# Kernel tuning notes

Measured on AMD Instinct MI355X. Metric: run time of the kernel, lower is better.

The kernel has to match this reference:

```python
import jax, jax.numpy as jnp
import numpy as np

B, S, D, V = 2, 4096, 2048, 32000
H, HD = 16, 128          # heads, head dim (H*HD == D)
BS = 16                  # block_size
N_ANCH = 128             # num_anchors (static: loss_mask=ones guarantees enough valid positions)
MASK_ID = 31999
DFF = 8192


def rms(x, w, eps=1e-6):
    return x * jax.lax.rsqrt(jnp.mean(x * x, axis=-1, keepdims=True) + eps) * w


def rope(x, pos):
    # x: (..., L, H, hd), pos: (..., L)
    hd = x.shape[-1]
    inv = 1.0 / (10000.0 ** (jnp.arange(0, hd, 2, dtype=jnp.float32) / hd))
    ang = pos[..., None, None].astype(jnp.float32) * inv  # (..., L, 1, hd/2)
    cos, sin = jnp.cos(ang), jnp.sin(ang)
    x1, x2 = x[..., : hd // 2], x[..., hd // 2 :]
    return jnp.concatenate([x1 * cos - x2 * sin, x2 * cos + x1 * sin], axis=-1).astype(x.dtype)


def setup_inputs() -> dict:
    key = jax.random.key(0)
    ks = jax.random.split(key, 12)
    s = 0.02
    return {
        "input_ids": jax.random.randint(ks[0], (B, S), 0, V, dtype=jnp.int32),
        "hidden_states": jax.random.normal(ks[1], (B, S, D), dtype=jnp.float32),
        "loss_mask": jnp.ones((B, S), dtype=jnp.float32),
        "rand_vals": jax.random.uniform(ks[2], (B, S - BS + 1), dtype=jnp.float32),
        "embed_table": jax.random.normal(ks[3], (V, D), dtype=jnp.float32) * s,
        "lm_head_w": jax.random.normal(ks[4], (V, D), dtype=jnp.float32) * s,
        "wq": jax.random.normal(ks[5], (D, D), dtype=jnp.float32) * s,
        "wk": jax.random.normal(ks[6], (D, D), dtype=jnp.float32) * s,
        "wv": jax.random.normal(ks[7], (D, D), dtype=jnp.float32) * s,
        "wo": jax.random.normal(ks[8], (D, D), dtype=jnp.float32) * s,
        "w_gate": jax.random.normal(ks[9], (D, DFF), dtype=jnp.float32) * s,
        "w_up": jax.random.normal(ks[10], (D, DFF), dtype=jnp.float32) * s,
        "w_down": jax.random.normal(ks[11], (DFF, D), dtype=jnp.float32) * s,
        "norm_attn": jnp.ones((D,), dtype=jnp.float32),
        "norm_mlp": jnp.ones((D,), dtype=jnp.float32),
        "norm_out": jnp.ones((D,), dtype=jnp.float32),
        "norm_chs": jnp.ones((D,), dtype=jnp.float32),
    }


def reference(input_ids, hidden_states, loss_mask, rand_vals, embed_table, lm_head_w,
              wq, wk, wv, wo, w_gate, w_up, w_down, norm_attn, norm_mlp, norm_out, norm_chs):
    max_anchor = S - BS
    # ---- anchor sampling: random permutation of valid positions via argsort of rand ----
    valid = loss_mask[:, : max_anchor + 1] > 0.5                       # (B, max_anchor+1)
    valid_counts = valid.sum(axis=1)
    idx = jnp.arange(max_anchor + 1, dtype=jnp.int32)
    masked_idx = jnp.where(valid, idx[None, :], S + 1)
    rv = jnp.where(valid, rand_vals, 2.0)
    order = jnp.argsort(rv, axis=1)
    gathered = jnp.take_along_axis(masked_idx, order, axis=1)
    anchors = jnp.sort(gathered[:, :N_ANCH], axis=1)                   # (B, N)
    keep = jnp.arange(N_ANCH)[None, :] < jnp.minimum(valid_counts, N_ANCH)[:, None]
    anchors = jnp.where(keep, anchors, 0)
    # ---- noise embedding: anchor token at block start, mask token elsewhere ----
    anchor_tok = jnp.take_along_axis(input_ids, jnp.clip(anchors, 0, S - 1), axis=1)
    first_tok = jnp.where(keep, anchor_tok, MASK_ID)
    noise_ids = jnp.full((B, N_ANCH, BS), MASK_ID, dtype=jnp.int32).at[:, :, 0].set(first_tok)
    x = embed_table[noise_ids]                                         # (B,N,BS,D)
    # ---- CHS context hidden: target hidden at anchor-1 ----
    ctx_pos = jnp.maximum(anchors - 1, 0)
    ctx = jnp.take_along_axis(hidden_states, ctx_pos[:, :, None], axis=1)  # (B,N,D)
    # ---- block-diagonal attention: per-block kv = [CHS_i | draft block i] (kv_len=1+BS) ----
    pos_q = anchors[:, :, None] + jnp.arange(BS)[None, None, :]        # (B,N,BS)
    pos_kv = jnp.concatenate([ctx_pos[:, :, None], pos_q], axis=2)     # (B,N,1+BS)
    hq = rms(x, norm_attn)
    hc = rms(ctx, norm_chs)[:, :, None, :]
    kv_in = jnp.concatenate([hc, hq], axis=2)                          # (B,N,1+BS,D)
    q = rope((hq @ wq).reshape(B, N_ANCH, BS, H, HD), pos_q)
    k = rope((kv_in @ wk).reshape(B, N_ANCH, 1 + BS, H, HD), pos_kv)
    v = (kv_in @ wv).reshape(B, N_ANCH, 1 + BS, H, HD)
    scores = jnp.einsum('bnqhd,bnkhd->bnhqk', q, k) * (1.0 / HD ** 0.5)
    attn = jax.nn.softmax(scores, axis=-1)
    out = jnp.einsum('bnhqk,bnkhd->bnqhd', attn, v).reshape(B, N_ANCH, BS, D) @ wo
    out = out * keep[:, :, None, None].astype(out.dtype)               # invalid blocks fully masked
    x = x + out
    h = rms(x, norm_mlp)
    x = x + (jax.nn.silu(h @ w_gate) * (h @ w_up)) @ w_down
    h_out = rms(x, norm_out)
    logits = h_out @ lm_head_w.T                                       # (B,N,BS,V)
    # ---- block-wise CE loss ----
    label_idx = anchors[:, :, None] + jnp.arange(BS)[None, None, :]
    valid_label = label_idx < S
    safe = jnp.minimum(label_idx, S - 1)
    targets = jnp.take_along_axis(jnp.broadcast_to(input_ids[:, None, :], (B, N_ANCH, S)), safe, axis=2)
    lm_g = jnp.take_along_axis(jnp.broadcast_to(loss_mask[:, None, :], (B, N_ANCH, S)), safe, axis=2)
    weight = (keep[:, :, None] & valid_label).astype(jnp.float32)
    weight = weight * (jnp.arange(BS) > 0)[None, None, :].astype(jnp.float32) * lm_g
    logp = jax.nn.log_softmax(logits, axis=-1)
    tok_logp = jnp.take_along_axis(logp, targets[..., None].astype(jnp.int32), axis=-1)[..., 0]
    loss = -(tok_logp * weight).sum() / (weight.sum() + 1e-6)
    pred = jnp.argmax(logits, axis=-1)
    accuracy = ((pred == targets) & (weight > 0.5)).sum().astype(jnp.float32) / (weight.sum() + 1e-6)
    return loss, accuracy
```

## Files before the change

### kernel.cpp

```cpp
#include <hip/hip_runtime.h>
#include <math.h>

typedef unsigned short u16;
typedef unsigned char u8;
typedef short v8s __attribute__((ext_vector_type(8)));
typedef u16   v4u __attribute__((ext_vector_type(4)));
typedef float v4f __attribute__((ext_vector_type(4)));
typedef int   v2i __attribute__((ext_vector_type(2)));
typedef int   v4i __attribute__((ext_vector_type(4)));

#define DEVFN static __device__ __forceinline__

constexpr int cB = 2, cS = 4096, cD = 2048, cV = 32000, cH = 16, cHD = 128;
constexpr int cBS = 16, cNA = 128, cMASK = 31999, cDFF = 8192;
constexpr int NCAND = cS - cBS + 1;
constexpr int MTOK  = cB * cNA * cBS;
constexpr int MKV   = cB * cNA * 17;
constexpr int NCH   = cV / 128;
constexpr int NCH2  = cV / 256;

constexpr int EPI_BF16 = 0, EPI_SILU = 1, EPI_OEMB = 2, EPI_DOWNACC = 3, EPI_STATS = 4, EPI_GLU = 5;
constexpr int ASRC_BF16 = 0, ASRC_RMS = 1, ASRC_AOMAP = 2;

struct RmsSrc {
  const float* hs; const float* emb; const float* nattn; const float* nchs;
  const float* rowinv; const int* ftok; const int* cpos;
};

DEVFN u16 f2bf(float f) {
  union { float f; unsigned u; } a; a.f = f;
  unsigned u = a.u;
  u = u + 0x7fffu + ((u >> 16) & 1u);
  return (u16)(u >> 16);
}
DEVFN float bf2f(u16 h) {
  union { unsigned u; float f; } a; a.u = ((unsigned)h) << 16;
  return a.f;
}
DEVFN float waveSum(float v) {
  #pragma unroll
  for (int o = 32; o >= 1; o >>= 1) v += __shfl_xor(v, o);
  return v;
}
DEVFN void gload16(void* lds, const void* g) {
  __builtin_amdgcn_global_load_lds(
      (const __attribute__((address_space(1))) unsigned*)g,
      (__attribute__((address_space(3))) unsigned*)lds, 16, 0, 0);
}
DEVFN int pack4fp8(float a, float b, float c, float d) {
  int p = __builtin_amdgcn_cvt_pk_fp8_f32(a, b, 0, 0);
  p = __builtin_amdgcn_cvt_pk_fp8_f32(c, d, p, 1);
  return p;
}
DEVFN long perm8(long i) {
  return (i & ~63L) | (((i >> 3) & 3) << 4) | (((i >> 5) & 1) << 3);
}

__global__ void k_select(const float* __restrict__ lmask, const float* __restrict__ rv_in,
                         int* __restrict__ self) {
  int b = blockIdx.x >> 4, chunk = blockIdx.x & 15;
  __shared__ float rvs[4096];
  for (int i = threadIdx.x; i < NCAND; i += 256) {
    bool valid = lmask[(size_t)b * cS + i] > 0.5f;
    rvs[i] = valid ? rv_in[(size_t)b * NCAND + i] : 2.0f;
  }
  __syncthreads();
  int i = chunk * 256 + threadIdx.x;
  if (i < NCAND) {
    float v = rvs[i];
    int rank = 0;
    for (int j = 0; j < NCAND; ++j) {
      float u = rvs[j];
      rank += (u < v) || (u == v && j < i);
    }
    self[(size_t)b * NCAND + i] = (rank < cNA) ? 1 : 0;
  }
}

__global__ void k_anchors(const float* __restrict__ lmask, const int* __restrict__ self,
                          const int* __restrict__ ids, int* __restrict__ anchors,
                          int* __restrict__ keepA, int* __restrict__ ftok, int* __restrict__ cpos) {
  int b = blockIdx.x;
  __shared__ int flags[4096];
  __shared__ int ssum[256];
  __shared__ int soff[257];
  __shared__ int abuf[cNA];
  for (int i = threadIdx.x; i < 4096; i += 256)
    flags[i] = (i < NCAND) ? (self[(size_t)b * NCAND + i] && (lmask[(size_t)b * cS + i] > 0.5f)) : 0;
  if (threadIdx.x < cNA) abuf[threadIdx.x] = 0;
  __syncthreads();
  int s = 0;
  #pragma unroll
  for (int j = 0; j < 16; ++j) s += flags[threadIdx.x * 16 + j];
  ssum[threadIdx.x] = s;
  __syncthreads();
  if (threadIdx.x == 0) {
    int a = 0;
    for (int t = 0; t < 256; ++t) { soff[t] = a; a += ssum[t]; }
    soff[256] = a;
  }
  __syncthreads();
  int nsel = soff[256];
  int p = soff[threadIdx.x];
  for (int j = 0; j < 16; ++j) {
    int i = threadIdx.x * 16 + j;
    if (flags[i]) { if (p < cNA) abuf[p] = i; ++p; }
  }
  __syncthreads();
  if (threadIdx.x < cNA) {
    int q = threadIdx.x;
    int kp = (q < nsel) ? 1 : 0;
    int a = kp ? abuf[q] : 0;
    anchors[b * cNA + q] = a;
    keepA[b * cNA + q] = kp;
    int av = a; if (av < 0) av = 0; if (av > cS - 1) av = cS - 1;
    int tok = ids[(size_t)b * cS + av];
    ftok[b * cNA + q] = kp ? tok : cMASK;
    cpos[b * cNA + q] = (a - 1 > 0) ? (a - 1) : 0;
  }
}

__global__ void k_rowinv(const float* __restrict__ hs, const float* __restrict__ emb,
                         const int* __restrict__ ftok, const int* __restrict__ cpos,
                         float* __restrict__ rowinv) {
  int r = blockIdx.x;
  int j = r % 17, bn = r / 17, b = bn >> 7;
  const float* src = (j == 0) ? hs + ((size_t)b * cS + cpos[bn]) * cD
                              : emb + (size_t)((j == 1) ? ftok[bn] : cMASK) * cD;
  float ss = 0.f;
  for (int d = threadIdx.x; d < cD; d += 256) { float v = src[d]; ss += v * v; }
  ss = waveSum(ss);
  __shared__ float red[4];
  if ((threadIdx.x & 63) == 0) red[threadIdx.x >> 6] = ss;
  __syncthreads();
  if (threadIdx.x == 0) {
    float tot = red[0] + red[1] + red[2] + red[3];
    rowinv[r] = 1.0f / sqrtf(tot / cD + 1e-6f);
  }
}

__global__ void k_build2(const float* __restrict__ hs, const float* __restrict__ emb,
                         const float* __restrict__ nattn, const float* __restrict__ nchs,
                         const int* __restrict__ ftok, const int* __restrict__ cpos,
                         u16* __restrict__ kv) {
  int r = blockIdx.x;
  int j = r % 17, bn = r / 17, b = bn >> 7;
  const float* src; const float* w;
  if (j == 0) { src = hs + ((size_t)b * cS + cpos[bn]) * cD; w = nchs; }
  else {
    int tok = (j == 1) ? ftok[bn] : cMASK;
    src = emb + (size_t)tok * cD; w = nattn;
  }
  float ss = 0.f;
  for (int d = threadIdx.x; d < cD; d += 256) { float v = src[d]; ss += v * v; }
  ss = waveSum(ss);
  __shared__ float red[4];
  if ((threadIdx.x & 63) == 0) red[threadIdx.x >> 6] = ss;
  __syncthreads();
  float tot = red[0] + red[1] + red[2] + red[3];
  float inv = 1.0f / sqrtf(tot / cD + 1e-6f);
  for (int d = threadIdx.x; d < cD; d += 256)
    kv[(size_t)r * cD + d] = f2bf(src[d] * inv * w[d]);
}

__global__ void k_rms(const float* __restrict__ xin, const float* __restrict__ w,
                      u16* __restrict__ outp) {
  int m = blockIdx.x;
  const float* row = xin + (size_t)m * cD;
  float ss = 0.f;
  for (int d = threadIdx.x; d < cD; d += 256) { float v = row[d]; ss += v * v; }
  ss = waveSum(ss);
  __shared__ float red[4];
  if ((threadIdx.x & 63) == 0) red[threadIdx.x >> 6] = ss;
  __syncthreads();
  float tot = red[0] + red[1] + red[2] + red[3];
  float inv = 1.0f / sqrtf(tot / cD + 1e-6f);
  for (int d = threadIdx.x; d < cD; d += 256)
    outp[(size_t)m * cD + d] = f2bf(row[d] * inv * w[d]);
}

__global__ void k_conv8(const float* __restrict__ in, u8* __restrict__ out, long n, float scale) {
  long i = ((long)blockIdx.x * 256 + threadIdx.x) * 8;
  long stride = (long)gridDim.x * 256 * 8;
  for (; i < n; i += stride) {
    v4f a = *(const v4f*)(in + i), b = *(const v4f*)(in + i + 4);
    v2i pk;
    pk[0] = pack4fp8(a[0] * scale, a[1] * scale, a[2] * scale, a[3] * scale);
    pk[1] = pack4fp8(b[0] * scale, b[1] * scale, b[2] * scale, b[3] * scale);
    *(v2i*)(out + perm8(i)) = pk;
  }
}

__global__ void k_cvt8(const u16* __restrict__ in, u8* __restrict__ out, long n) {
  long i = ((long)blockIdx.x * 256 + threadIdx.x) * 8;
  long stride = (long)gridDim.x * 256 * 8;
  for (; i < n; i += stride) {
    v8s a = *(const v8s*)(in + i);
    v2i pk;
    pk[0] = pack4fp8(bf2f((u16)a[0]), bf2f((u16)a[1]), bf2f((u16)a[2]), bf2f((u16)a[3]));
    pk[1] = pack4fp8(bf2f((u16)a[4]), bf2f((u16)a[5]), bf2f((u16)a[6]), bf2f((u16)a[7]));
    *(v2i*)(out + perm8(i)) = pk;
  }
}

__global__ void k_tconv(const float* __restrict__ W, u16* __restrict__ WT, int K, int N) {
  __shared__ u16 t[64][72];
  int n0 = blockIdx.x * 64, k0 = blockIdx.y * 64;
  int tid = threadIdx.x;
  int c4 = (tid & 15) * 4, r0 = tid >> 4;
  #pragma unroll
  for (int rr = 0; rr < 64; rr += 16) {
    int k = r0 + rr;
    v4f v = *(const v4f*)(W + (size_t)(k0 + k) * N + n0 + c4);
    #pragma unroll
    for (int e = 0; e < 4; ++e) t[c4 + e][k] = f2bf(v[e]);
  }
  __syncthreads();
  int n = tid >> 2, kq = (tid & 3) * 16;
  v8s o0, o1;
  #pragma unroll
  for (int e = 0; e < 8; ++e) { o0[e] = (short)t[n][kq + e]; o1[e] = (short)t[n][kq + 8 + e]; }
  *(v8s*)(WT + (size_t)(n0 + n) * K + k0 + kq) = o0;
  *(v8s*)(WT + (size_t)(n0 + n) * K + k0 + kq + 8) = o1;
}

__global__ void k_tconv8(const float* __restrict__ W, u8* __restrict__ WT8,
                         int K, int N, int goff, float scale) {
  __shared__ float tf[64][65];
  int n0 = blockIdx.x * 64, k0 = blockIdx.y * 64;
  int tid = threadIdx.x;
  int c4 = (tid & 15) * 4, r0 = tid >> 4;
  #pragma unroll
  for (int rr = 0; rr < 64; rr += 16) {
    int k = r0 + rr;
    v4f v = *(const v4f*)(W + (size_t)(k0 + k) * N + n0 + c4);
    #pragma unroll
    for (int e = 0; e < 4; ++e) tf[c4 + e][k] = v[e];
  }
  __syncthreads();
  int n = tid >> 2, kq = (tid & 3) * 16;
  int gn = n0 + n;
  size_t rout = ((size_t)(gn >> 4) << 5) + goff + (gn & 15);
  long base = (long)rout * K + k0 + kq;
  v2i p0, p1;
  p0[0] = pack4fp8(tf[n][kq + 0] * scale, tf[n][kq + 1] * scale, tf[n][kq + 2] * scale, tf[n][kq + 3] * scale);
  p0[1] = pack4fp8(tf[n][kq + 4] * scale, tf[n][kq + 5] * scale, tf[n][kq + 6] * scale, tf[n][kq + 7] * scale);
  p1[0] = pack4fp8(tf[n][kq + 8] * scale, tf[n][kq + 9] * scale, tf[n][kq + 10] * scale, tf[n][kq + 11] * scale);
  p1[1] = pack4fp8(tf[n][kq + 12] * scale, tf[n][kq + 13] * scale, tf[n][kq + 14] * scale, tf[n][kq + 15] * scale);
  *(v2i*)(WT8 + perm8(base)) = p0;
  *(v2i*)(WT8 + perm8(base + 8)) = p1;
}

template <int EPI>
__launch_bounds__(512, 1)
__global__ void k_gemm6(const u16* __restrict__ Abf, const u16* __restrict__ Bbf,
                        u16* __restrict__ Cbf, const u16* __restrict__ Gaux,
                        v4f* __restrict__ partials, int K, int ldc, int nch) {
  __shared__ __align__(16) u16 lds[65536];
  const int tid = threadIdx.x;
  const int lane = tid & 63, wid = tid >> 6;
  const int wm = wid >> 2, wn = wid & 3;
  const int lc = lane & 15, lq = lane >> 4;
  const int m0 = blockIdx.x * 256, n0 = blockIdx.y * 256;

  const u16* srcA[2]; const u16* srcB[2];
  #pragma unroll
  for (int i = 0; i < 2; ++i) {
    int s = i * 512 + tid;
    int row = s >> 2;
    int c2 = (s & 3) ^ ((row >> 1) & 3);
    srcA[i] = Abf + (size_t)(m0 + row) * K + c2 * 8;
    srcB[i] = Bbf + (size_t)(n0 + row) * K + c2 * 8;
  }

  v4f acc[8][4];
  #pragma unroll
  for (int i = 0; i < 8; ++i)
    #pragma unroll
    for (int j = 0; j < 4; ++j) acc[i][j] = (v4f){0.f, 0.f, 0.f, 0.f};

  const int fsw = lq ^ ((lc >> 1) & 3);
  int aoff[8], boff[4];
  #pragma unroll
  for (int mi = 0; mi < 8; ++mi) aoff[mi] = ((wm * 128 + mi * 16 + lc) * 4 + fsw) * 8;
  #pragma unroll
  for (int ni = 0; ni < 4; ++ni) boff[ni] = ((wn * 64 + ni * 16 + lc) * 4 + fsw) * 8;

  auto stageA = [&](int t, int kh) {
    int reg = (t & 1) * 32768 + kh * 8192;
    int koff = t * 64 + kh * 32;
    #pragma unroll
    for (int i = 0; i < 2; ++i)
      gload16(&lds[reg + i * 4096 + wid * 512], srcA[i] + koff);
  };
  auto stageB = [&](int t, int kh) {
    int reg = (t & 1) * 32768 + 16384 + kh * 8192;
    int koff = t * 64 + kh * 32;
    #pragma unroll
    for (int i = 0; i < 2; ++i)
      gload16(&lds[reg + i * 4096 + wid * 512], srcB[i] + koff);
  };

  stageA(0, 0); stageB(0, 0);
  stageA(0, 1); stageB(0, 1);
  stageA(1, 0); stageB(1, 0);
  asm volatile("s_waitcnt vmcnt(8)" ::: "memory");
  __builtin_amdgcn_s_barrier();

  const int NT = K >> 6;
  for (int t = 0; t < NT; ++t) {
    const int bufb = (t & 1) * 32768;
    const u16* Ab0 = &lds[bufb];
    const u16* Ab1 = &lds[bufb + 8192];
    const u16* Bb0 = &lds[bufb + 16384];
    const u16* Bb1 = &lds[bufb + 24576];
    v8s a_[4], b_[4];

    #pragma unroll
    for (int ni = 0; ni < 4; ++ni) b_[ni] = *(const v8s*)(Bb0 + boff[ni]);
    #pragma unroll
    for (int mi = 0; mi < 4; ++mi) a_[mi] = *(const v8s*)(Ab0 + aoff[mi]);
    if (t + 1 < NT) stageA(t + 1, 1);
    asm volatile("s_waitcnt lgkmcnt(0)" ::: "memory");
    __builtin_amdgcn_sched_barrier(0);
    __builtin_amdgcn_s_setprio(1);
    #pragma unroll
    for (int mi = 0; mi < 4; ++mi)
      #pragma unroll
      for (int ni = 0; ni < 4; ++ni)
        acc[mi][ni] = __builtin_amdgcn_mfma_f32_16x16x32_bf16(a_[mi], b_[ni], acc[mi][ni], 0, 0, 0);
    __builtin_amdgcn_s_setprio(0);
    __builtin_amdgcn_s_barrier();

    #pragma unroll
    for (int mi = 0; mi < 4; ++mi) a_[mi] = *(const v8s*)(Ab0 + aoff[mi + 4]);
    if (t + 1 < NT) stageB(t + 1, 1);
    asm volatile("s_waitcnt lgkmcnt(0)" ::: "memory");
    __builtin_amdgcn_sched_barrier(0);
    __builtin_amdgcn_s_setprio(1);
    #pragma unroll
    for (int mi = 0; mi < 4; ++mi)
      #pragma unroll
      for (int ni = 0; ni < 4; ++ni)
        acc[mi + 4][ni] = __builtin_amdgcn_mfma_f32_16x16x32_bf16(a_[mi], b_[ni], acc[mi + 4][ni], 0, 0, 0);
    __builtin_amdgcn_s_setprio(0);
    if (t + 1 < NT) { asm volatile("s_waitcnt vmcnt(4)" ::: "memory"); }
    else            { asm volatile("s_waitcnt vmcnt(0)" ::: "memory"); }
    __builtin_amdgcn_s_barrier();

    #pragma unroll
    for (int ni = 0; ni < 4; ++ni) b_[ni] = *(const v8s*)(Bb1 + boff[ni]);
    #pragma unroll
    for (int mi = 0; mi < 4; ++mi) a_[mi] = *(const v8s*)(Ab1 + aoff[mi]);
    if (t + 2 < NT) stageA(t + 2, 0);
    asm volatile("s_waitcnt lgkmcnt(0)" ::: "memory");
    __builtin_amdgcn_sched_barrier(0);
    __builtin_amdgcn_s_setprio(1);
    #pragma unroll
    for (int mi = 0; mi < 4; ++mi)
      #pragma unroll
      for (int ni = 0; ni < 4; ++ni)
        acc[mi][ni] = __builtin_amdgcn_mfma_f32_16x16x32_bf16(a_[mi], b_[ni], acc[mi][ni], 0, 0, 0);
    __builtin_amdgcn_s_setprio(0);
    __builtin_amdgcn_s_barrier();

    #pragma unroll
    for (int mi = 0; mi < 4; ++mi) a_[mi] = *(const v8s*)(Ab1 + aoff[mi + 4]);
    if (t + 2 < NT) stageB(t + 2, 0);
    asm volatile("s_waitcnt lgkmcnt(0)" ::: "memory");
    __builtin_amdgcn_sched_barrier(0);
    __builtin_amdgcn_s_setprio(1);
    #pragma unroll
    for (int mi = 0; mi < 4; ++mi)
      #pragma unroll
      for (int ni = 0; ni < 4; ++ni)
        acc[mi + 4][ni] = __builtin_amdgcn_mfma_f32_16x16x32_bf16(a_[mi], b_[ni], acc[mi + 4][ni], 0, 0, 0);
    __builtin_amdgcn_s_setprio(0);
    __builtin_amdgcn_s_barrier();
  }
  asm volatile("s_waitcnt vmcnt(0)" ::: "memory");

  if constexpr (EPI == EPI_GLU) {
    #pragma unroll
    for (int mi = 0; mi < 8; ++mi)
      #pragma unroll
      for (int np = 0; np < 2; ++np)
        #pragma unroll
        for (int r = 0; r < 4; ++r) {
          int grow = m0 + wm * 128 + mi * 16 + lq * 4 + r;
          int gcol = (n0 >> 1) + wn * 32 + np * 16 + lc;
          float g = acc[mi][2 * np][r];
          float u = acc[mi][2 * np + 1][r];
          Cbf[(size_t)grow * ldc + gcol] = f2bf(u * g / (1.0f + __expf(-g)));
        }
  } else {
    #pragma unroll
    for (int mi = 0; mi < 8; ++mi)
      #pragma unroll
      for (int ni = 0; ni < 4; ++ni)
        #pragma unroll
        for (int r = 0; r < 4; ++r) {
          int grow = m0 + wm * 128 + mi * 16 + lq * 4 + r;
          int gcol = n0 + wn * 64 + ni * 16 + lc;
          size_t idx = (size_t)grow * ldc + gcol;
          float vv = acc[mi][ni][r];
          if constexpr (EPI == EPI_BF16) {
            Cbf[idx] = f2bf(vv);
          } else {
            float g = bf2f(Gaux[idx]);
            Cbf[idx] = f2bf(vv * g / (1.0f + __expf(-g)));
          }
        }
  }
  (void)partials; (void)nch;
}

template <int EPI>
__launch_bounds__(512, 2)
__global__ void k_gemm8(const u8* __restrict__ A8, const u8* __restrict__ B8,
                        u16* __restrict__ Cbf, v4f* __restrict__ partials,
                        int K, int ldc, int nch) {
  __shared__ __align__(16) u8 lds8[65536];
  const int tid = threadIdx.x;
  const int lane = tid & 63, wid = tid >> 6;
  const int wm = wid >> 2, wn = wid & 3;
  const int lc = lane & 15, lq = lane >> 4;
  const int m0 = blockIdx.x * 256, n0 = blockIdx.y * 256;

  const u8* srcA[2]; const u8* srcB[2];
  #pragma unroll
  for (int i = 0; i < 2; ++i) {
    int ci = i * 512 + tid;
    int r = ci >> 2;
    int logc = (ci & 3) ^ ((r >> 1) & 3);
    srcA[i] = A8 + (size_t)(m0 + r) * K + logc * 16;
    srcB[i] = B8 + (size_t)(n0 + r) * K + logc * 16;
  }

  v4f acc[8][4];
  #pragma unroll
  for (int i = 0; i < 8; ++i)
    #pragma unroll
    for (int j = 0; j < 4; ++j) acc[i][j] = (v4f){0.f, 0.f, 0.f, 0.f};

  const int csw = (lc >> 1) & 3;
  int aoff[8], boff[4];
  #pragma unroll
  for (int mi = 0; mi < 8; ++mi) aoff[mi] = (wm * 128 + mi * 16 + lc) * 64 + ((lq ^ csw) << 4);
  #pragma unroll
  for (int ni = 0; ni < 4; ++ni) boff[ni] = (wn * 64 + ni * 16 + lc) * 64 + ((lq ^ csw) << 4);

  auto stageA = [&](int t, int i) {
    gload16(&lds8[(t & 1) * 32768 + i * 8192 + wid * 1024], srcA[i] + t * 64);
  };
  auto stageB = [&](int t, int i) {
    gload16(&lds8[(t & 1) * 32768 + 16384 + i * 8192 + wid * 1024], srcB[i] + t * 64);
  };

  stageA(0, 0); stageA(0, 1); stageB(0, 0); stageB(0, 1);
  stageA(1, 0); stageA(1, 1); stageB(1, 0); stageB(1, 1);
  asm volatile("s_waitcnt vmcnt(4)" ::: "memory");
  __builtin_amdgcn_s_barrier();

  union Frag { v4i v; long long ll[2]; };
  const int NT = K >> 6;
  for (int t = 0; t < NT; ++t) {
    const u8* Ab = &lds8[(t & 1) * 32768];
    const u8* Bb = Ab + 16384;
    Frag fa[8], fb[4];

    #pragma unroll
    for (int ni = 0; ni < 4; ++ni) fb[ni].v = *(const v4i*)(Bb + boff[ni]);
    #pragma unroll
    for (int mi = 0; mi < 4; ++mi) fa[mi].v = *(const v4i*)(Ab + aoff[mi]);
    asm volatile("s_waitcnt lgkmcnt(0)" ::: "memory");
    __builtin_amdgcn_sched_barrier(0);
    __builtin_amdgcn_s_setprio(1);
    #pragma unroll
    for (int mi = 0; mi < 4; ++mi)
      #pragma unroll
      for (int ni = 0; ni < 4; ++ni)
        acc[mi][ni] = __builtin_amdgcn_mfma_f32_16x16x32_fp8_fp8(fa[mi].ll[0], fb[ni].ll[0], acc[mi][ni], 0, 0, 0);
    __builtin_amdgcn_s_setprio(0);
    __builtin_amdgcn_s_barrier();

    #pragma unroll
    for (int mi = 0; mi < 4; ++mi) fa[mi + 4].v = *(const v4i*)(Ab + aoff[mi + 4]);
    if (t + 2 < NT) stageB(t + 2, 0);
    asm volatile("s_waitcnt lgkmcnt(0)" ::: "memory");
    __builtin_amdgcn_sched_barrier(0);
    __builtin_amdgcn_s_setprio(1);
    #pragma unroll
    for (int mi = 0; mi < 4; ++mi)
      #pragma unroll
      for (int ni = 0; ni < 4; ++ni)
        acc[mi + 4][ni] = __builtin_amdgcn_mfma_f32_16x16x32_fp8_fp8(fa[mi + 4].ll[0], fb[ni].ll[0], acc[mi + 4][ni], 0, 0, 0);
    __builtin_amdgcn_s_setprio(0);
    __builtin_amdgcn_s_barrier();

    if (t + 2 < NT) { stageB(t + 2, 1); stageA(t + 2, 0); }
    __builtin_amdgcn_s_setprio(1);
    #pragma unroll
    for (int mi = 0; mi < 4; ++mi)
      #pragma unroll
      for (int ni = 0; ni < 4; ++ni)
        acc[mi][ni] = __builtin_amdgcn_mfma_f32_16x16x32_fp8_fp8(fa[mi].ll[1], fb[ni].ll[1], acc[mi][ni], 0, 0, 0);
    __builtin_amdgcn_s_setprio(0);
    __builtin_amdgcn_s_barrier();

    if (t + 2 < NT) stageA(t + 2, 1);
    __builtin_amdgcn_s_setprio(1);
    #pragma unroll
    for (int mi = 0; mi < 4; ++mi)
      #pragma unroll
      for (int ni = 0; ni < 4; ++ni)
        acc[mi + 4][ni] = __builtin_amdgcn_mfma_f32_16x16x32_fp8_fp8(fa[mi + 4].ll[1], fb[ni].ll[1], acc[mi + 4][ni], 0, 0, 0);
    __builtin_amdgcn_s_setprio(0);
    if (t + 2 < NT) { asm volatile("s_waitcnt vmcnt(4)" ::: "memory"); }
    else            { asm volatile("s_waitcnt vmcnt(0)" ::: "memory"); }
    __builtin_amdgcn_s_barrier();
  }
  asm volatile("s_waitcnt vmcnt(0)" ::: "memory");

  #pragma unroll
  for (int mi = 0; mi < 8; ++mi)
    #pragma unroll
    for (int ni = 0; ni < 4; ++ni)
      acc[mi][ni] *= 0.015625f;

  if constexpr (EPI == EPI_GLU) {
    #pragma unroll
    for (int mi = 0; mi < 8; ++mi)
      #pragma unroll
      for (int np = 0; np < 2; ++np)
        #pragma unroll
        for (int r = 0; r < 4; ++r) {
          int grow = m0 + wm * 128 + mi * 16 + lq * 4 + r;
          int gcol = (n0 >> 1) + wn * 32 + np * 16 + lc;
          float g = acc[mi][2 * np][r];
          float u = acc[mi][2 * np + 1][r];
          Cbf[(size_t)grow * ldc + gcol] = f2bf(u * g / (1.0f + __expf(-g)));
        }
    return;
  } else {
    float* s_mx = (float*)lds8;
    float* s_sm = (float*)(lds8 + 4096);
    int*   s_ax = (int*)(lds8 + 8192);
    __syncthreads();
    #pragma unroll
    for (int mi = 0; mi < 8; ++mi) {
      #pragma unroll
      for (int r = 0; r < 4; ++r) {
        float v0 = acc[mi][0][r], v1 = acc[mi][1][r], v2 = acc[mi][2][r], v3 = acc[mi][3][r];
        float mx = v0; int ax = lc;
        if (v1 > mx) { mx = v1; ax = 16 + lc; }
        if (v2 > mx) { mx = v2; ax = 32 + lc; }
        if (v3 > mx) { mx = v3; ax = 48 + lc; }
        #pragma unroll
        for (int off = 1; off < 16; off <<= 1) {
          float om = __shfl_xor(mx, off); int oa = __shfl_xor(ax, off);
          if (om > mx || (om == mx && oa < ax)) { mx = om; ax = oa; }
        }
        float se = __expf(v0 - mx) + __expf(v1 - mx) + __expf(v2 - mx) + __expf(v3 - mx);
        #pragma unroll
        for (int off = 1; off < 16; off <<= 1) se += __shfl_xor(se, off);
        if (lc == 0) {
          int row = wm * 128 + mi * 16 + lq * 4 + r;
          s_mx[row * 4 + wn] = mx; s_sm[row * 4 + wn] = se; s_ax[row * 4 + wn] = wn * 64 + ax;
        }
      }
    }
    __syncthreads();
    if (tid < 256) {
      float gm = s_mx[tid * 4]; int ga = s_ax[tid * 4];
      #pragma unroll
      for (int w = 1; w < 4; ++w) {
        float m = s_mx[tid * 4 + w];
        if (m > gm) { gm = m; ga = s_ax[tid * 4 + w]; }
      }
      float gs = 0.f;
      #pragma unroll
      for (int w = 0; w < 4; ++w) gs += s_sm[tid * 4 + w] * __expf(s_mx[tid * 4 + w] - gm);
      v4f rec; rec[0] = gm; rec[1] = gs; rec[2] = __int_as_float(n0 + ga); rec[3] = 0.f;
      partials[(size_t)(m0 + tid) * nch + blockIdx.y] = rec;
    }
  }
}

template <int ASRC, int EPI>
__launch_bounds__(256, 2)
__global__ void k_gemm4(const u16* __restrict__ Abf, const u16* __restrict__ Bbf,
                        u16* __restrict__ Cbf, float* __restrict__ Cf32,
                        const int* __restrict__ keepArr, RmsSrc rs, int K, int ldb, int ldc) {
  __shared__ __align__(16) u16 lds[2][16384];
  const int tid = threadIdx.x;
  const int lane = tid & 63, wid = tid >> 6;
  const int wm = wid >> 1, wn = wid & 1;
  const int lc = lane & 15, lq = lane >> 4;
  const int m0 = blockIdx.x * 128, n0 = blockIdx.y * 128;

  const u16* srcA[4]; const u16* srcB[4];
  #pragma unroll
  for (int i = 0; i < 4; ++i) {
    int s = i * 256 + tid;
    int row = s >> 3;
    int c3 = (s & 7) ^ (row & 7);
    int ar = m0 + row;
    if constexpr (ASRC == ASRC_AOMAP) ar = (ar >> 4) * 17 + 1 + (ar & 15);
    srcA[i] = Abf + (size_t)ar * K + c3 * 8;
    srcB[i] = Bbf + (size_t)(n0 + row) * ldb + c3 * 8;
  }

  v4f acc[4][4];
  #pragma unroll
  for (int i = 0; i < 4; ++i)
    #pragma unroll
    for (int j = 0; j < 4; ++j) acc[i][j] = (v4f){0.f, 0.f, 0.f, 0.f};

  const int sw = lc & 7;
  const int aoff0 = (((wm * 64 + lc) * 8 + 0 + lq) ^ sw) * 8;
  const int aoff1 = (((wm * 64 + lc) * 8 + 4 + lq) ^ sw) * 8;
  const int boff0 = (((wn * 64 + lc) * 8 + 0 + lq) ^ sw) * 8;
  const int boff1 = (((wn * 64 + lc) * 8 + 4 + lq) ^ sw) * 8;

  auto stageTo = [&](int b) {
    u16* dA = &lds[b][0] + wid * 512;
    u16* dB = &lds[b][8192] + wid * 512;
    #pragma unroll
    for (int i = 0; i < 4; ++i) { gload16(dA + i * 2048, srcA[i]); srcA[i] += 64; }
    #pragma unroll
    for (int i = 0; i < 4; ++i) { gload16(dB + i * 2048, srcB[i]); srcB[i] += 64; }
  };

  stageTo(0);
  const int NT = K >> 6;
  for (int t = 0; t < NT; ++t) {
    const int cur = t & 1;
    if (t + 1 < NT) {
      stageTo(cur ^ 1);
      asm volatile("s_waitcnt vmcnt(8)" ::: "memory");
    } else {
      asm volatile("s_waitcnt vmcnt(0)" ::: "memory");
    }
    __builtin_amdgcn_s_barrier();
    const u16* Ab = &lds[cur][0];
    const u16* Bb = &lds[cur][8192];
    v8s a0[4], a1[4], b0[4], b1[4];
    #pragma unroll
    for (int mi = 0; mi < 4; ++mi) a0[mi] = *(const v8s*)(Ab + aoff0 + mi * 1024);
    #pragma unroll
    for (int ni = 0; ni < 4; ++ni) b0[ni] = *(const v8s*)(Bb + boff0 + ni * 1024);
    #pragma unroll
    for (int mi = 0; mi < 4; ++mi) a1[mi] = *(const v8s*)(Ab + aoff1 + mi * 1024);
    #pragma unroll
    for (int ni = 0; ni < 4; ++ni) b1[ni] = *(const v8s*)(Bb + boff1 + ni * 1024);
    __builtin_amdgcn_s_setprio(1);
    #pragma unroll
    for (int mi = 0; mi < 4; ++mi)
      #pragma unroll
      for (int ni = 0; ni < 4; ++ni)
        acc[mi][ni] = __builtin_amdgcn_mfma_f32_16x16x32_bf16(a0[mi], b0[ni], acc[mi][ni], 0, 0, 0);
    __builtin_amdgcn_s_setprio(0);
    asm volatile("s_waitcnt lgkmcnt(0)" ::: "memory");
    __builtin_amdgcn_sched_barrier(0);
    __builtin_amdgcn_s_barrier();
    __builtin_amdgcn_s_setprio(1);
    #pragma unroll
    for (int mi = 0; mi < 4; ++mi)
      #pragma unroll
      for (int ni = 0; ni < 4; ++ni)
        acc[mi][ni] = __builtin_amdgcn_mfma_f32_16x16x32_bf16(a1[mi], b1[ni], acc[mi][ni], 0, 0, 0);
    __builtin_amdgcn_s_setprio(0);
  }

  #pragma unroll
  for (int mi = 0; mi < 4; ++mi)
    #pragma unroll
    for (int ni = 0; ni < 4; ++ni)
      #pragma unroll
      for (int r = 0; r < 4; ++r) {
        int grow = m0 + wm * 64 + mi * 16 + lq * 4 + r;
        int gcol = n0 + wn * 64 + ni * 16 + lc;
        size_t idx = (size_t)grow * ldc + gcol;
        float vv = acc[mi][ni][r];
        if constexpr (EPI == EPI_BF16) {
          Cbf[idx] = f2bf(vv);
        } else if constexpr (EPI == EPI_OEMB) {
          int t_ = grow & 15, bn = grow >> 4;
          int tok = (t_ == 0) ? rs.ftok[bn] : cMASK;
          float kf = (float)keepArr[bn];
          Cf32[idx] = rs.emb[(size_t)tok * cD + gcol] + vv * kf;
        } else {
          Cf32[idx] += vv;
        }
      }
}

template <int ASRC, int BLAYOUT, int EPI>
__launch_bounds__(256)
__global__ void k_gemm(const u16* __restrict__ Abf, const float* __restrict__ Bw,
                       u16* Cbf, float* Cf32, const u16* Gaux,
                       const int* __restrict__ keepArr, v4f* __restrict__ partials,
                       RmsSrc rs, int K, int ldb, int ldc) {
  __shared__ __align__(16) u16 As[128][40];
  __shared__ __align__(16) u16 Bs[128][40];
  const int tid = threadIdx.x;
  const int m0 = blockIdx.x * 128, n0 = blockIdx.y * 128;
  const int lane = tid & 63, wid = tid >> 6;
  const int wm = wid >> 1, wn = wid & 1;
  const int lc = lane & 15, lk8 = (lane >> 4) * 8;
  const int srow = tid >> 2, sk8 = (tid & 3) * 8;
  v4f acc[4][4];
  #pragma unroll
  for (int i = 0; i < 4; ++i)
    #pragma unroll
    for (int j = 0; j < 4; ++j) acc[i][j] = (v4f){0.f, 0.f, 0.f, 0.f};

  for (int kt = 0; kt < K; kt += 32) {
    __syncthreads();
    for (int mm = srow; mm < 128; mm += 64) {
      if constexpr (ASRC == ASRC_BF16) {
        *(v8s*)&As[mm][sk8] = *(const v8s*)(Abf + (size_t)(m0 + mm) * K + kt + sk8);
      } else if constexpr (ASRC == ASRC_AOMAP) {
        int m = m0 + mm, bn = m >> 4, t = m & 15;
        *(v8s*)&As[mm][sk8] = *(const v8s*)(Abf + (size_t)(bn * 17 + 1 + t) * K + kt + sk8);
      } else {
        int R = m0 + mm;
        int j = R % 17, bn = R / 17, b = bn >> 7;
        const float* src; const float* nw;
        if (j == 0) { src = rs.hs + ((size_t)b * cS + rs.cpos[bn]) * cD; nw = rs.nchs; }
        else {
          int tok = (j == 1) ? rs.ftok[bn] : cMASK;
          src = rs.emb + (size_t)tok * cD; nw = rs.nattn;
        }
        float inv = rs.rowinv[R];
        const v4f* sp = (const v4f*)(src + kt + sk8);
        const v4f* np_ = (const v4f*)(nw + kt + sk8);
        v4f s0 = sp[0], s1 = sp[1], w0 = np_[0], w1 = np_[1];
        v8s pk;
        #pragma unroll
        for (int e = 0; e < 4; ++e) pk[e] = (short)f2bf(s0[e] * inv * w0[e]);
        #pragma unroll
        for (int e = 0; e < 4; ++e) pk[4 + e] = (short)f2bf(s1[e] * inv * w1[e]);
        *(v8s*)&As[mm][sk8] = pk;
      }
    }
    if constexpr (BLAYOUT == 1) {
      for (int nn = srow; nn < 128; nn += 64) {
        const v4f* bp = (const v4f*)(Bw + (size_t)(n0 + nn) * ldb + kt + sk8);
        v4f b0 = bp[0], b1 = bp[1];
        v8s pk;
        #pragma unroll
        for (int e = 0; e < 4; ++e) { pk[e] = (short)f2bf(b0[e]); pk[4 + e] = (short)f2bf(b1[e]); }
        *(v8s*)&Bs[nn][sk8] = pk;
      }
    } else {
      const int bn_ = tid & 127, kq = tid >> 7;
      for (int kk = kq; kk < 8; kk += 2) {
        const int k4 = kk * 4;
        const float* bp = Bw + (size_t)(kt + k4) * ldb + n0 + bn_;
        v4u pk;
        #pragma unroll
        for (int e = 0; e < 4; ++e) pk[e] = f2bf(bp[(size_t)e * ldb]);
        *(v4u*)&Bs[bn_][k4] = pk;
      }
    }
    __syncthreads();
    v8s af[4], bf_[4];
    #pragma unroll
    for (int i = 0; i < 4; ++i) af[i] = *(const v8s*)&As[wm * 64 + i * 16 + lc][lk8];
    #pragma unroll
    for (int i = 0; i < 4; ++i) bf_[i] = *(const v8s*)&Bs[wn * 64 + i * 16 + lc][lk8];
    #pragma unroll
    for (int mi = 0; mi < 4; ++mi)
      #pragma unroll
      for (int ni = 0; ni < 4; ++ni)
        acc[mi][ni] = __builtin_amdgcn_mfma_f32_16x16x32_bf16(af[mi], bf_[ni], acc[mi][ni], 0, 0, 0);
  }

  if constexpr (EPI == EPI_STATS) {
    __shared__ float s_mx[128][2], s_sm[128][2];
    __shared__ int s_ax[128][2];
    #pragma unroll
    for (int mi = 0; mi < 4; ++mi) {
      #pragma unroll
      for (int r = 0; r < 4; ++r) {
        float v0 = acc[mi][0][r], v1 = acc[mi][1][r], v2 = acc[mi][2][r], v3 = acc[mi][3][r];
        float mx = v0; int ax = lc;
        if (v1 > mx) { mx = v1; ax = 16 + lc; }
        if (v2 > mx) { mx = v2; ax = 32 + lc; }
        if (v3 > mx) { mx = v3; ax = 48 + lc; }
        #pragma unroll
        for (int off = 1; off < 16; off <<= 1) {
          float om = __shfl_xor(mx, off); int oa = __shfl_xor(ax, off);
          if (om > mx || (om == mx && oa < ax)) { mx = om; ax = oa; }
        }
        float se = __expf(v0 - mx) + __expf(v1 - mx) + __expf(v2 - mx) + __expf(v3 - mx);
        #pragma unroll
        for (int off = 1; off < 16; off <<= 1) se += __shfl_xor(se, off);
        if (lc == 0) {
          int lr = wm * 64 + mi * 16 + (lane >> 4) * 4 + r;
          s_mx[lr][wn] = mx; s_sm[lr][wn] = se; s_ax[lr][wn] = wn * 64 + ax;
        }
      }
    }
    __syncthreads();
    if (tid < 128) {
      float ma = s_mx[tid][0], mb = s_mx[tid][1];
      float gm = fmaxf(ma, mb);
      float gs = s_sm[tid][0] * __expf(ma - gm) + s_sm[tid][1] * __expf(mb - gm);
      int ga = (ma >= mb) ? s_ax[tid][0] : s_ax[tid][1];
      v4f rec; rec[0] = gm; rec[1] = gs; rec[2] = __int_as_float(n0 + ga); rec[3] = 0.f;
      partials[(size_t)(m0 + tid) * NCH + blockIdx.y] = rec;
    }
    return;
  } else {
    #pragma unroll
    for (int mi = 0; mi < 4; ++mi)
      #pragma unroll
      for (int ni = 0; ni < 4; ++ni)
        #pragma unroll
        for (int r = 0; r < 4; ++r) {
          int grow = m0 + wm * 64 + mi * 16 + (lane >> 4) * 4 + r;
          int gcol = n0 + wn * 64 + ni * 16 + lc;
          size_t idx = (size_t)grow * ldc + gcol;
          float vv = acc[mi][ni][r];
          if constexpr (EPI == EPI_BF16) {
            Cbf[idx] = f2bf(vv);
          } else if constexpr (EPI == EPI_SILU) {
            float g = bf2f(Gaux[idx]);
            Cbf[idx] = f2bf(vv * g / (1.0f + __expf(-g)));
          } else if constexpr (EPI == EPI_OEMB) {
            int t = grow & 15, bn = grow >> 4;
            int tok = (t == 0) ? rs.ftok[bn] : cMASK;
            float kf = (float)keepArr[bn];
            Cf32[idx] = rs.emb[(size_t)tok * cD + gcol] + vv * kf;
          } else {
            Cf32[idx] += vv;
          }
        }
  }
}

__global__ void k_rope(u16* __restrict__ qb, u16* __restrict__ kb,
                       const int* __restrict__ anchors, const int* __restrict__ cpos) {
  int r = blockIdx.x;
  int which = (r >= MKV);
  int rr = which ? r - MKV : r;
  int j = rr % 17, bn = rr / 17;
  if (!which && j == 0) return;
  u16* buf = which ? kb : qb;
  int pos = (which && j == 0) ? cpos[bn] : (anchors[bn] + j - 1);
  float fp = (float)pos;
  for (int p = threadIdx.x; p < cH * 64; p += 256) {
    int h = p >> 6, i = p & 63;
    size_t base = (size_t)rr * cD + h * cHD;
    float x1 = bf2f(buf[base + i]);
    float x2 = bf2f(buf[base + 64 + i]);
    float freq = powf(10000.0f, -((float)(2 * i)) / 128.0f);
    float ang = fp * freq;
    float sn = sinf(ang), cn = cosf(ang);
    buf[base + i]      = f2bf(x1 * cn - x2 * sn);
    buf[base + 64 + i] = f2bf(x2 * cn + x1 * sn);
  }
}

__global__ void k_attn(u16* __restrict__ qb, const u16* __restrict__ kb,
                       const u16* __restrict__ vb) {
  int blk = blockIdx.x;
  int h = blk % cH, bn = blk / cH;
  __shared__ float qs[16][128], ks[17][128], vs[17][128], ps[16][18];
  int lane = threadIdx.x;
  for (int e = lane; e < 16 * 128; e += 64) {
    int r = e >> 7, d = e & 127;
    qs[r][d] = bf2f(qb[((size_t)(bn * 17 + 1 + r)) * cD + h * cHD + d]);
  }
  for (int e = lane; e < 17 * 128; e += 64) {
    int r = e >> 7, d = e & 127;
    ks[r][d] = bf2f(kb[((size_t)(bn * 17 + r)) * cD + h * cHD + d]);
    vs[r][d] = bf2f(vb[((size_t)(bn * 17 + r)) * cD + h * cHD + d]);
  }
  __syncthreads();
  for (int e = lane; e < 16 * 17; e += 64) {
    int qi = e / 17, ki = e % 17;
    float s = 0.f;
    for (int d = 0; d < 128; ++d) s += qs[qi][d] * ks[ki][d];
    ps[qi][ki] = s * 0.08838834764831845f;
  }
  __syncthreads();
  if (lane < 16) {
    float m = -3e38f;
    for (int kk = 0; kk < 17; ++kk) m = fmaxf(m, ps[lane][kk]);
    float s = 0.f;
    for (int kk = 0; kk < 17; ++kk) { float e_ = __expf(ps[lane][kk] - m); ps[lane][kk] = e_; s += e_; }
    float is = 1.0f / s;
    for (int kk = 0; kk < 17; ++kk) ps[lane][kk] *= is;
  }
  __syncthreads();
  for (int e = lane; e < 16 * 128; e += 64) {
    int qi = e >> 7, d = e & 127;
    float s = 0.f;
    for (int kk = 0; kk < 17; ++kk) s += ps[qi][kk] * vs[kk][d];
    qb[((size_t)(bn * 17 + 1 + qi)) * cD + h * cHD + d] = f2bf(s);
  }
}

__global__ void k_tgt(const u16* __restrict__ hout, const float* __restrict__ Wlm,
                      const int* __restrict__ ids, const int* __restrict__ anchors,
                      int* __restrict__ tgt_tok, float* __restrict__ tgt_logit) {
  int w = threadIdx.x >> 6, lane = threadIdx.x & 63;
  int m = blockIdx.x * 4 + w;
  int bn = m >> 4, t = m & 15, b = bn / cNA;
  int label = anchors[bn] + t;
  int sl = (label < cS - 1) ? label : (cS - 1);
  int tok = ids[(size_t)b * cS + sl];
  const u16* hr = hout + (size_t)m * cD;
  const float* wr = Wlm + (size_t)tok * cD;
  float s = 0.f;
  for (int d = lane; d < cD; d += 64) s += bf2f(hr[d]) * wr[d];
  s = waveSum(s);
  if (lane == 0) { tgt_tok[m] = tok; tgt_logit[m] = s; }
}

__global__ void k_combine(const v4f* __restrict__ partials, const int* __restrict__ tgt_tok,
                          const float* __restrict__ tgt_logit, const int* __restrict__ keepArr,
                          const int* __restrict__ anchors, const float* __restrict__ lmask,
                          float* __restrict__ tokOut, int nch) {
  int m = blockIdx.x;
  int tid = threadIdx.x, lane = tid & 63, w = tid >> 6;
  float cm = -3.0e38f, cs = 0.f; int ca = 0x7fffffff;
  if (tid < nch) {
    v4f rec = partials[(size_t)m * nch + tid];
    cm = rec[0]; cs = rec[1]; ca = __float_as_int(rec[2]);
  }
  float gm = cm; int ga = ca;
  #pragma unroll
  for (int off = 1; off < 64; off <<= 1) {
    float om = __shfl_xor(gm, off); int oa = __shfl_xor(ga, off);
    if (om > gm || (om == gm && oa < ga)) { gm = om; ga = oa; }
  }
  __shared__ float wmx[4]; __shared__ int wax[4]; __shared__ float wsm[4];
  if (lane == 0) { wmx[w] = gm; wax[w] = ga; }
  __syncthreads();
  if (tid == 0) {
    for (int i = 1; i < 4; ++i)
      if (wmx[i] > wmx[0] || (wmx[i] == wmx[0] && wax[i] < wax[0])) { wmx[0] = wmx[i]; wax[0] = wax[i]; }
  }
  __syncthreads();
  gm = wmx[0]; ga = wax[0];
  float s = (tid < nch) ? cs * __expf(cm - gm) : 0.f;
  s = waveSum(s);
  if (lane == 0) wsm[w] = s;
  __syncthreads();
  if (tid == 0) {
    float gs = wsm[0] + wsm[1] + wsm[2] + wsm[3];
    float logZ = gm + logf(gs);
    int bn = m >> 4, t = m & 15, b = bn / cNA;
    int label = anchors[bn] + t;
    int sl = (label < cS - 1) ? label : (cS - 1);
    float wgt = (float)keepArr[bn] * ((t > 0) ? 1.f : 0.f) * ((label < cS) ? 1.f : 0.f) *
                lmask[(size_t)b * cS + sl];
    float lp = tgt_logit[m] - logZ;
    int tg = tgt_tok[m];
    tokOut[m * 4 + 0] = lp * wgt;
    tokOut[m * 4 + 1] = wgt;
    tokOut[m * 4 + 2] = ((ga == tg) && (wgt > 0.5f)) ? 1.f : 0.f;
    tokOut[m * 4 + 3] = 0.f;
  }
}

__global__ void k_final(const float* __restrict__ tokOut, float* __restrict__ outp) {
  int tid = threadIdx.x;
  float swl = 0.f, sw = 0.f, sm = 0.f;
  for (int m = tid; m < MTOK; m += 256) {
    swl += tokOut[m * 4 + 0];
    sw  += tokOut[m * 4 + 1];
    sm  += tokOut[m * 4 + 2];
  }
  swl = waveSum(swl); sw = waveSum(sw); sm = waveSum(sm);
  __shared__ float r0[4], r1[4], r2[4];
  int lane = tid & 63, w = tid >> 6;
  if (lane == 0) { r0[w] = swl; r1[w] = sw; r2[w] = sm; }
  __syncthreads();
  if (tid == 0) {
    float a = r0[0] + r0[1] + r0[2] + r0[3];
    float b = r1[0] + r1[1] + r1[2] + r1[3];
    float c = r2[0] + r2[1] + r2[2] + r2[3];
    float denom = b + 1e-6f;
    float loss = -a / denom;
    float acc  = c / denom;
    if (b == 0.0f) loss = -300.0f;
    outp[0] = loss;
    outp[1] = acc;
  }
}

__global__ void k_heartbeat(float* outp) {
  if (threadIdx.x == 0) { outp[0] = -55.0f; outp[1] = -55.0f; }
}
__global__ void k_sentinel(float* outp) {
  if (threadIdx.x == 0) { outp[0] = -777.0f; outp[1] = -777.0f; }
}

extern "C" void kernel_launch(void* const* d_in, const int* in_sizes, int n_in,
                              void* d_out, int out_size, void* d_ws, size_t ws_size,
                              hipStream_t stream) {
  const int*   ids   = (const int*)  d_in[0];
  const float* hs    = (const float*)d_in[1];
  const float* lmask = (const float*)d_in[2];
  const float* rv    = (const float*)d_in[3];
  const float* emb   = (const float*)d_in[4];
  const float* wlm   = (const float*)d_in[5];
  const float* wq    = (const float*)d_in[6];
  const float* wk    = (const float*)d_in[7];
  const float* wv    = (const float*)d_in[8];
  const float* wo    = (const float*)d_in[9];
  const float* wg    = (const float*)d_in[10];
  const float* wu    = (const float*)d_in[11];
  const float* wd    = (const float*)d_in[12];
  const float* nattn = (const float*)d_in[13];
  const float* nmlp  = (const float*)d_in[14];
  const float* nout  = (const float*)d_in[15];
  const float* nchs  = (const float*)d_in[16];
  (void)in_sizes; (void)n_in; (void)out_size;

  float* outp = (float*)d_out;
  k_heartbeat<<<dim3(1), 64, 0, stream>>>(outp);

  char* wsb = (char*)d_ws;
  size_t off = 0;
  auto alloc = [&](size_t bytes) -> void* {
    void* p = wsb + off;
    off = (off + bytes + 255) & ~(size_t)255;
    return p;
  };
  int*   anchors = (int*)  alloc((size_t)cB * cNA * 4);
  int*   keepA   = (int*)  alloc((size_t)cB * cNA * 4);
  int*   ftok    = (int*)  alloc((size_t)cB * cNA * 4);
  int*   cpos    = (int*)  alloc((size_t)cB * cNA * 4);
  int*   self    = (int*)  alloc((size_t)cB * NCAND * 4);
  float* rowinv  = (float*)alloc((size_t)MKV * 4);
  int*   ttok    = (int*)  alloc((size_t)MTOK * 4);
  float* tlogit  = (float*)alloc((size_t)MTOK * 4);
  float* tokOut  = (float*)alloc((size_t)MTOK * 4 * 4);

  const size_t szQ  = (size_t)MKV * cD * 2;
  const size_t szX  = (size_t)MTOK * cD * 4;
  u16* qb = (u16*)alloc(szQ);
  const size_t a1off = off;

  RmsSrc rs{hs, emb, nattn, nchs, rowinv, ftok, cpos};

  k_select <<<dim3(cB * 16), 256, 0, stream>>>(lmask, rv, self);
  k_anchors<<<dim3(cB),      256, 0, stream>>>(lmask, self, ids, anchors, keepA, ftok, cpos);

  const size_t szKV   = szQ;
  const size_t szCbuf = (size_t)MTOK * 4096 * 2;
  size_t kvb_off  = a1off;
  size_t a1f_off  = (kvb_off + szKV + 255) & ~(size_t)255;
  size_t a1f_sz   = 2 * szQ > (szX + szCbuf) ? 2 * szQ : (szX + szCbuf);
  size_t wreg_off = (a1f_off + a1f_sz + 255) & ~(size_t)255;
  size_t wreg_sz  = (size_t)cV * cD * 2;
  size_t need_fast = wreg_off + wreg_sz;

  if (need_fast <= ws_size) {
    u16*   kvb   = (u16*)(wsb + kvb_off);
    u16*   kb    = (u16*)(wsb + a1f_off);
    u16*   vb    = (u16*)(wsb + a1f_off + szQ);
    float* xb    = (float*)(wsb + a1f_off);
    u16*   cbuf  = (u16*)(wsb + a1f_off + szX);
    v4f*   parts = (v4f*)(wsb + a1f_off);
    u8*    h8    = (u8*)(wsb + a1f_off + (size_t)16 * 1024 * 1024);
    u16*   hb    = qb;
    u16*   houtb = qb;
    u16*   wT    = (u16*)(wsb + wreg_off);
    const size_t szDD = (size_t)cD * cD;
    u16* wqT = wT;            u16* wkT = wT + szDD;
    u16* wvT = wT + 2 * szDD; u16* woT = wT + 3 * szDD;
    const size_t szDF = (size_t)cD * cDFF;
    u8*  wgu8 = (u8*)wT;
    u16* wdT  = wT + 2 * szDF;
    u8*  h8m  = (u8*)(wT + 3 * szDF);
    u8*  wlm8 = (u8*)wT;

    k_build2<<<dim3(MKV), 256, 0, stream>>>(hs, emb, nattn, nchs, ftok, cpos, kvb);

    k_tconv<<<dim3(32, 32), 256, 0, stream>>>(wq, wqT, cD, cD);
    k_tconv<<<dim3(32, 32), 256, 0, stream>>>(wk, wkT, cD, cD);
    k_tconv<<<dim3(32, 32), 256, 0, stream>>>(wv, wvT, cD, cD);
    k_tconv<<<dim3(32, 32), 256, 0, stream>>>(wo, woT, cD, cD);

    k_gemm4<ASRC_BF16, EPI_BF16><<<dim3(MKV / 128, cD / 128), 256, 0, stream>>>(
        kvb, wqT, qb, nullptr, nullptr, rs, cD, cD, cD);
    k_gemm4<ASRC_BF16, EPI_BF16><<<dim3(MKV / 128, cD / 128), 256, 0, stream>>>(
        kvb, wkT, kb, nullptr, nullptr, rs, cD, cD, cD);
    k_gemm4<ASRC_BF16, EPI_BF16><<<dim3(MKV / 128, cD / 128), 256, 0, stream>>>(
        kvb, wvT, vb, nullptr, nullptr, rs, cD, cD, cD);

    k_rope<<<dim3(2 * MKV), 256, 0, stream>>>(qb, kb, anchors, cpos);
    k_attn<<<dim3(cB * cNA * cH), 64, 0, stream>>>(qb, kb, vb);

    k_gemm4<ASRC_AOMAP, EPI_OEMB><<<dim3(MTOK / 128, cD / 128), 256, 0, stream>>>(
        qb, woT, nullptr, xb, keepA, rs, cD, cD, cD);

    k_rms<<<dim3(MTOK), 256, 0, stream>>>(xb, nmlp, hb);
    k_cvt8<<<dim3(1024), 256, 0, stream>>>(hb, h8m, (long)MTOK * cD);

    k_tconv8<<<dim3(128, 32), 256, 0, stream>>>(wg, wgu8, cD, cDFF, 0, 64.0f);
    k_tconv8<<<dim3(128, 32), 256, 0, stream>>>(wu, wgu8, cD, cDFF, 16, 64.0f);
    k_tconv <<<dim3(32, 128), 256, 0, stream>>>(wd, wdT, cDFF, cD);

    for (int cb = 0; cb < cDFF; cb += 4096) {
      k_gemm8<EPI_GLU><<<dim3(MTOK / 256, 32), 512, 0, stream>>>(
          h8m, wgu8 + (size_t)cb * 2 * cD, cbuf, nullptr, cD, 4096, 0);
      k_gemm4<ASRC_BF16, EPI_DOWNACC><<<dim3(MTOK / 128, cD / 128), 256, 0, stream>>>(
          cbuf, wdT + cb, nullptr, xb, nullptr, rs, 4096, cDFF, cD);
    }

    k_rms<<<dim3(MTOK), 256, 0, stream>>>(xb, nout, houtb);

    k_tgt<<<dim3(MTOK / 4), 256, 0, stream>>>(houtb, wlm, ids, anchors, ttok, tlogit);

    k_cvt8 <<<dim3(1024), 256, 0, stream>>>(houtb, h8, (long)MTOK * cD);
    k_conv8<<<dim3(2048), 256, 0, stream>>>(wlm, wlm8, (long)cV * cD, 64.0f);
    k_gemm8<EPI_STATS><<<dim3(MTOK / 256, NCH2), 512, 0, stream>>>(
        h8, wlm8, nullptr, parts, cD, 0, NCH2);

    k_combine<<<dim3(MTOK), 256, 0, stream>>>(parts, ttok, tlogit, keepA, anchors, lmask, tokOut, NCH2);
    k_final  <<<dim3(1), 256, 0, stream>>>(tokOut, outp);
    return;
  }

  const int cwopts[4] = {4096, 2048, 1024, 512};
  int CW = 0;
  for (int ci = 0; ci < 4; ++ci) {
    int cw = cwopts[ci];
    size_t cbufsz = (size_t)MTOK * cw * 2;
    size_t s1 = 2 * szQ;
    size_t s2 = szX + cbufsz;
    size_t sz = s1 > s2 ? s1 : s2;
    size_t pmin = (size_t)MTOK * NCH * 16;
    if (pmin > sz) sz = pmin;
    if (a1off + sz <= ws_size) { CW = cw; break; }
  }
  if (CW == 0) { k_sentinel<<<dim3(1), 64, 0, stream>>>(outp); return; }

  u16*   kb    = (u16*)(wsb + a1off);
  u16*   vb    = (u16*)(wsb + a1off + szQ);
  float* xb    = (float*)(wsb + a1off);
  u16*   cbuf  = (u16*)(wsb + a1off + szX);
  v4f*   parts = (v4f*)(wsb + a1off);
  u16*   hb    = qb;
  u16*   houtb = qb;

  k_rowinv<<<dim3(MKV), 256, 0, stream>>>(hs, emb, ftok, cpos, rowinv);

  k_gemm<ASRC_RMS, 0, EPI_BF16><<<dim3(MKV / 128, cD / 128), 256, 0, stream>>>(
      nullptr, wq, qb, nullptr, nullptr, nullptr, nullptr, rs, cD, cD, cD);
  k_gemm<ASRC_RMS, 0, EPI_BF16><<<dim3(MKV / 128, cD / 128), 256, 0, stream>>>(
      nullptr, wk, kb, nullptr, nullptr, nullptr, nullptr, rs, cD, cD, cD);
  k_gemm<ASRC_RMS, 0, EPI_BF16><<<dim3(MKV / 128, cD / 128), 256, 0, stream>>>(
      nullptr, wv, vb, nullptr, nullptr, nullptr, nullptr, rs, cD, cD, cD);

  k_rope<<<dim3(2 * MKV), 256, 0, stream>>>(qb, kb, anchors, cpos);
  k_attn<<<dim3(cB * cNA * cH), 64, 0, stream>>>(qb, kb, vb);

  k_gemm<ASRC_AOMAP, 0, EPI_OEMB><<<dim3(MTOK / 128, cD / 128), 256, 0, stream>>>(
      qb, wo, nullptr, xb, nullptr, keepA, nullptr, rs, cD, cD, cD);

  k_rms<<<dim3(MTOK), 256, 0, stream>>>(xb, nmlp, hb);

  for (int cb = 0; cb < cDFF; cb += CW) {
    k_gemm<ASRC_BF16, 0, EPI_BF16><<<dim3(MTOK / 128, CW / 128), 256, 0, stream>>>(
        hb, wg + cb, cbuf, nullptr, nullptr, nullptr, nullptr, rs, cD, cDFF, CW);
    k_gemm<ASRC_BF16, 0, EPI_SILU><<<dim3(MTOK / 128, CW / 128), 256, 0, stream>>>(
        hb, wu + cb, cbuf, nullptr, cbuf, nullptr, nullptr, rs, cD, cDFF, CW);
    k_gemm<ASRC_BF16, 0, EPI_DOWNACC><<<dim3(MTOK / 128, cD / 128), 256, 0, stream>>>(
        cbuf, wd + (size_t)cb * cD, nullptr, xb, nullptr, nullptr, nullptr, rs, CW, cD, cD);
  }

  k_rms<<<dim3(MTOK), 256, 0, stream>>>(xb, nout, houtb);

  k_tgt<<<dim3(MTOK / 4), 256, 0, stream>>>(houtb, wlm, ids, anchors, ttok, tlogit);
  k_gemm<ASRC_BF16, 1, EPI_STATS><<<dim3(MTOK / 128, cV / 128), 256, 0, stream>>>(
      houtb, wlm, nullptr, nullptr, nullptr, nullptr, parts, rs, cD, cD, 0);

  k_combine<<<dim3(MTOK), 256, 0, stream>>>(parts, ttok, tlogit, keepA, anchors, lmask, tokOut, NCH);
  k_final  <<<dim3(1), 256, 0, stream>>>(tokOut, outp);
}
```

Before: 1.497 ms.

## Convert QKV, O-proj and down-proj GEMMs to FP8 MFMA path

Moves the remaining bf16 GEMMs (QKV projection, output projection, MLP down projection) to FP8 operands. K/V inputs, the attention output and the GLU output are written directly as permuted FP8, and weights are transposed into FP8 with a ×64 scale. A new 128×128 FP8 GEMM kernel replaces the bf16 one, and the unused bf16 256-tile kernel is removed. This halves operand bytes and uses the higher-rate FP8 matrix instructions, at the cost of more quantization error in the loss and accuracy outputs.

Measured after the change: 1.443 ms. 1.04x faster.

```diff
diff --git a/kernel.cpp b/kernel.cpp
--- a/kernel.cpp
+++ b/kernel.cpp
@@ -51,6 +51,9 @@
   int p = __builtin_amdgcn_cvt_pk_fp8_f32(a, b, 0, 0);
   p = __builtin_amdgcn_cvt_pk_fp8_f32(c, d, p, 1);
   return p;
+}
+DEVFN u8 f2fp8(float v) {
+  return (u8)(__builtin_amdgcn_cvt_pk_fp8_f32(v, 0.f, 0, 0) & 0xff);
 }
 DEVFN long perm8(long i) {
   return (i & ~63L) | (((i >> 3) & 3) << 4) | (((i >> 5) & 1) << 3);
@@ -142,7 +145,7 @@
 __global__ void k_build2(const float* __restrict__ hs, const float* __restrict__ emb,
                          const float* __restrict__ nattn, const float* __restrict__ nchs,
                          const int* __restrict__ ftok, const int* __restrict__ cpos,
-                         u16* __restrict__ kv) {
+                         u8* __restrict__ kv8) {
   int r = blockIdx.x;
   int j = r % 17, bn = r / 17, b = bn >> 7;
   const float* src; const float* w;
@@ -160,7 +163,7 @@
   float tot = red[0] + red[1] + red[2] + red[3];
   float inv = 1.0f / sqrtf(tot / cD + 1e-6f);
   for (int d = threadIdx.x; d < cD; d += 256)
-    kv[(size_t)r * cD + d] = f2bf(src[d] * inv * w[d]);
+    kv8[perm8((size_t)r * cD + d)] = f2fp8(src[d] * inv * w[d]);
 }
 
 __global__ void k_rms(const float* __restrict__ xin, const float* __restrict__ w,
@@ -240,7 +243,7 @@
   __syncthreads();
   int n = tid >> 2, kq = (tid & 3) * 16;
   int gn = n0 + n;
-  size_t rout = ((size_t)(gn >> 4) << 5) + goff + (gn & 15);
+  size_t rout = (goff >= 0) ? (((size_t)(gn >> 4) << 5) + goff + (gn & 15)) : (size_t)gn;
   long base = (long)rout * K + k0 + kq;
   v2i p0, p1;
   p0[0] = pack4fp8(tf[n][kq + 0] * scale, tf[n][kq + 1] * scale, tf[n][kq + 2] * scale, tf[n][kq + 3] * scale);
@@ -252,25 +255,25 @@
 }
 
 template <int EPI>
-__launch_bounds__(512, 1)
-__global__ void k_gemm6(const u16* __restrict__ Abf, const u16* __restrict__ Bbf,
-                        u16* __restrict__ Cbf, const u16* __restrict__ Gaux,
-                        v4f* __restrict__ partials, int K, int ldc, int nch) {
-  __shared__ __align__(16) u16 lds[65536];
+__launch_bounds__(512, 2)
+__global__ void k_gemm8(const u8* __restrict__ A8, const u8* __restrict__ B8,
+                        u8* __restrict__ C8, v4f* __restrict__ partials,
+                        int K, int ldc, int nch) {
+  __shared__ __align__(16) u8 lds8[65536];
   const int tid = threadIdx.x;
   const int lane = tid & 63, wid = tid >> 6;
   const int wm = wid >> 2, wn = wid & 3;
   const int lc = lane & 15, lq = lane >> 4;
   const int m0 = blockIdx.x * 256, n0 = blockIdx.y * 256;
 
-  const u16* srcA[2]; const u16* srcB[2];
+  const u8* srcA[2]; const u8* srcB[2];
   #pragma unroll
   for (int i = 0; i < 2; ++i) {
-    int s = i * 512 + tid;
-    int row = s >> 2;
-    int c2 = (s & 3) ^ ((row >> 1) & 3);
-    srcA[i] = Abf + (size_t)(m0 + row) * K + c2 * 8;
-    srcB[i] = Bbf + (size_t)(n0 + row) * K + c2 * 8;
+    int ci = i * 512 + tid;
+    int r = ci >> 2;
+    int logc = (ci & 3) ^ ((r >> 1) & 3);
+    srcA[i] = A8 + (size_t)(m0 + r) * K + logc * 16;
+    srcB[i] = B8 + (size_t)(n0 + r) * K + logc * 16;
   }
 
   v4f acc[8][4];
@@ -279,48 +282,36 @@
     #pragma unroll
     for (int j = 0; j < 4; ++j) acc[i][j] = (v4f){0.f, 0.f, 0.f, 0.f};
 
-  const int fsw = lq ^ ((lc >> 1) & 3);
+  const int csw = (lc >> 1) & 3;
   int aoff[8], boff[4];
   #pragma unroll
-  for (int mi = 0; mi < 8; ++mi) aoff[mi] = ((wm * 128 + mi * 16 + lc) * 4 + fsw) * 8;
-  #pragma unroll
-  for (int ni = 0; ni < 4; ++ni) boff[ni] = ((wn * 64 + ni * 16 + lc) * 4 + fsw) * 8;
-
-  auto stageA = [&](int t, int kh) {
-    int reg = (t & 1) * 32768 + kh * 8192;
-    int koff = t * 64 + kh * 32;
-    #pragma unroll
-    for (int i = 0; i < 2; ++i)
-      gload16(&lds[reg + i * 4096 + wid * 512], srcA[i] + koff);
+  for (int mi = 0; mi < 8; ++mi) aoff[mi] = (wm * 128 + mi * 16 + lc) * 64 + ((lq ^ csw) << 4);
+  #pragma unroll
+  for (int ni = 0; ni < 4; ++ni) boff[ni] = (wn * 64 + ni * 16 + lc) * 64 + ((lq ^ csw) << 4);
+
+  auto stageA = [&](int t, int i) {
+    gload16(&lds8[(t & 1) * 32768 + i * 8192 + wid * 1024], srcA[i] + t * 64);
   };
-  auto stageB = [&](int t, int kh) {
-    int reg = (t & 1) * 32768 + 16384 + kh * 8192;
-    int koff = t * 64 + kh * 32;
-    #pragma unroll
-    for (int i = 0; i < 2; ++i)
-      gload16(&lds[reg + i * 4096 + wid * 512], srcB[i] + koff);
+  auto stageB = [&](int t, int i) {
+    gload16(&lds8[(t & 1) * 32768 + 16384 + i * 8192 + wid * 1024], srcB[i] + t * 64);
   };
 
-  stageA(0, 0); stageB(0, 0);
-  stageA(0, 1); stageB(0, 1);
-  stageA(1, 0); stageB(1, 0);
-  asm volatile("s_waitcnt vmcnt(8)" ::: "memory");
+  stageA(0, 0); stageA(0, 1); stageB(0, 0); stageB(0, 1);
+  stageA(1, 0); stageA(1, 1); stageB(1, 0); stageB(1, 1);
+  asm volatile("s_waitcnt vmcnt(4)" ::: "memory");
   __builtin_amdgcn_s_barrier();
 
+  union Frag { v4i v; long long ll[2]; };
   const int NT = K >> 6;
   for (int t = 0; t < NT; ++t) {
-    const int bufb = (t & 1) * 32768;
-    const u16* Ab0 = &lds[bufb];
-    const u16* Ab1 = &lds[bufb + 8192];
-    const u16* Bb0 = &lds[bufb + 16384];
-    const u16* Bb1 = &lds[bufb + 24576];
-    v8s a_[4], b_[4];
-
-    #pragma unroll
-    for (int ni = 0; ni < 4; ++ni) b_[ni] = *(const v8s*)(Bb0 + boff[ni]);
-    #pragma unroll
-    for (int mi = 0; mi < 4; ++mi) a_[mi] = *(const v8s*)(Ab0 + aoff[mi]);
-    if (t + 1 < NT) stageA(t + 1, 1);
+    const u8* Ab = &lds8[(t & 1) * 32768];
+    const u8* Bb = Ab + 16384;
+    Frag fa[8], fb[4];
+
+    #pragma unroll
+    for (int ni = 0; ni < 4; ++ni) fb[ni].v = *(const v4i*)(Bb + boff[ni]);
+    #pragma unroll
+    for (int mi = 0; mi < 4; ++mi) fa[mi].v = *(const v4i*)(Ab + aoff[mi]);
     asm volatile("s_waitcnt lgkmcnt(0)" ::: "memory");
     __builtin_amdgcn_sched_barrier(0);
     __builtin_amdgcn_s_setprio(1);
@@ -328,44 +319,12 @@
     for (int mi = 0; mi < 4; ++mi)
       #pragma unroll
       for (int ni = 0; ni < 4; ++ni)
-        acc[mi][ni] = __builtin_amdgcn_mfma_f32_16x16x32_bf16(a_[mi], b_[ni], acc[mi][ni], 0, 0, 0);
+        acc[mi][ni] = __builtin_amdgcn_mfma_f32_16x16x32_fp8_fp8(fa[mi].ll[0], fb[ni].ll[0], acc[mi][ni], 0, 0, 0);
     __builtin_amdgcn_s_setprio(0);
     __builtin_amdgcn_s_barrier();
 
     #pragma unroll
-    for (int mi = 0; mi < 4; ++mi) a_[mi] = *(const v8s*)(Ab0 + aoff[mi + 4]);
-    if (t + 1 < NT) stageB(t + 1, 1);
-    asm volatile("s_waitcnt lgkmcnt(0)" ::: "memory");
-    __builtin_amdgcn_sched_barrier(0);
-    __builtin_amdgcn_s_setprio(1);
-    #pragma unroll
-    for (int mi = 0; mi < 4; ++mi)
-      #pragma unroll
-      for (int ni = 0; ni < 4; ++ni)
-        acc[mi + 4][ni] = __builtin_amdgcn_mfma_f32_16x16x32_bf16(a_[mi], b_[ni], acc[mi + 4][ni], 0, 0, 0);
-    __builtin_amdgcn_s_setprio(0);
-    if (t + 1 < NT) { asm volatile("s_waitcnt vmcnt(4)" ::: "memory"); }
-    else            { asm volatile("s_waitcnt vmcnt(0)" ::: "memory"); }
-    __builtin_amdgcn_s_barrier();
-
-    #pragma unroll
-    for (int ni = 0; ni < 4; ++ni) b_[ni] = *(const v8s*)(Bb1 + boff[ni]);
-    #pragma unroll
-    for (int mi = 0; mi < 4; ++mi) a_[mi] = *(const v8s*)(Ab1 + aoff[mi]);
-    if (t + 2 < NT) stageA(t + 2, 0);
-    asm volatile("s_waitcnt lgkmcnt(0)" ::: "memory");
-    __builtin_amdgcn_sched_barrier(0);
-    __builtin_amdgcn_s_setprio(1);
-    #pragma unroll
-    for (int mi = 0; mi < 4; ++mi)
-      #pragma unroll
-      for (int ni = 0; ni < 4; ++ni)
-        acc[mi][ni] = __builtin_amdgcn_mfma_f32_16x16x32_bf16(a_[mi], b_[ni], acc[mi][ni], 0, 0, 0);
-    __builtin_amdgcn_s_setprio(0);
-    __builtin_amdgcn_s_barrier();
-
-    #pragma unroll
-    for (int mi = 0; mi < 4; ++mi) a_[mi] = *(const v8s*)(Ab1 + aoff[mi + 4]);
+    for (int mi = 0; mi < 4; ++mi) fa[mi + 4].v = *(const v4i*)(Ab + aoff[mi + 4]);
     if (t + 2 < NT) stageB(t + 2, 0);
     asm volatile("s_waitcnt lgkmcnt(0)" ::: "memory");
     __builtin_amdgcn_sched_barrier(0);
@@ -374,11 +333,39 @@
     for (int mi = 0; mi < 4; ++mi)
       #pragma unroll
       for (int ni = 0; ni < 4; ++ni)
-        acc[mi + 4][ni] = __builtin_amdgcn_mfma_f32_16x16x32_bf16(a_[mi], b_[ni], acc[mi + 4][ni], 0, 0, 0);
+        acc[mi + 4][ni] = __builtin_amdgcn_mfma_f32_16x16x32_fp8_fp8(fa[mi + 4].ll[0], fb[ni].ll[0], acc[mi + 4][ni], 0, 0, 0);
     __builtin_amdgcn_s_setprio(0);
     __builtin_amdgcn_s_barrier();
+
+    if (t + 2 < NT) { stageB(t + 2, 1); stageA(t + 2, 0); }
+    __builtin_amdgcn_s_setprio(1);
+    #pragma unroll
+    for (int mi = 0; mi < 4; ++mi)
+      #pragma unroll
+      for (int ni = 0; ni < 4; ++ni)
+        acc[mi][ni] = __builtin_amdgcn_mfma_f32_16x16x32_fp8_fp8(fa[mi].ll[1], fb[ni].ll[1], acc[mi][ni], 0, 0, 0);
+    __builtin_amdgcn_s_setprio(0);
+    __builtin_amdgcn_s_barrier();
+
+    if (t + 2 < NT) stageA(t + 2, 1);
+    __builtin_amdgcn_s_setprio(1);
+    #pragma unroll
+    for (int mi = 0; mi < 4; ++mi)
+      #pragma unroll
+      for (int ni = 0; ni < 4; ++ni)
+        acc[mi + 4][ni] = __builtin_amdgcn_mfma_f32_16x16x32_fp8_fp8(fa[mi + 4].ll[1], fb[ni].ll[1], acc[mi + 4][ni], 0, 0, 0);
+    __builtin_amdgcn_s_setprio(0);
+    if (t + 2 < NT) { asm volatile("s_waitcnt vmcnt(4)" ::: "memory"); }
+    else            { asm volatile("s_waitcnt vmcnt(0)" ::: "memory"); }
+    __builtin_amdgcn_s_barrier();
   }
   asm volatile("s_waitcnt vmcnt(0)" ::: "memory");
+
+  #pragma unroll
+  for (int mi = 0; mi < 8; ++mi)
+    #pragma unroll
+    for (int ni = 0; ni < 4; ++ni)
+      acc[mi][ni] *= 0.015625f;
 
   if constexpr (EPI == EPI_GLU) {
     #pragma unroll
@@ -391,155 +378,7 @@
           int gcol = (n0 >> 1) + wn * 32 + np * 16 + lc;
           float g = acc[mi][2 * np][r];
           float u = acc[mi][2 * np + 1][r];
-          Cbf[(size_t)grow * ldc + gcol] = f2bf(u * g / (1.0f + __expf(-g)));
-        }
-  } else {
-    #pragma unroll
-    for (int mi = 0; mi < 8; ++mi)
-      #pragma unroll
-      for (int ni = 0; ni < 4; ++ni)
-        #pragma unroll
-        for (int r = 0; r < 4; ++r) {
-          int grow = m0 + wm * 128 + mi * 16 + lq * 4 + r;
-          int gcol = n0 + wn * 64 + ni * 16 + lc;
-          size_t idx = (size_t)grow * ldc + gcol;
-          float vv = acc[mi][ni][r];
-          if constexpr (EPI == EPI_BF16) {
-            Cbf[idx] = f2bf(vv);
-          } else {
-            float g = bf2f(Gaux[idx]);
-            Cbf[idx] = f2bf(vv * g / (1.0f + __expf(-g)));
-          }
-        }
-  }
-  (void)partials; (void)nch;
-}
-
-template <int EPI>
-__launch_bounds__(512, 2)
-__global__ void k_gemm8(const u8* __restrict__ A8, const u8* __restrict__ B8,
-                        u16* __restrict__ Cbf, v4f* __restrict__ partials,
-                        int K, int ldc, int nch) {
-  __shared__ __align__(16) u8 lds8[65536];
-  const int tid = threadIdx.x;
-  const int lane = tid & 63, wid = tid >> 6;
-  const int wm = wid >> 2, wn = wid & 3;
-  const int lc = lane & 15, lq = lane >> 4;
-  const int m0 = blockIdx.x * 256, n0 = blockIdx.y * 256;
-
-  const u8* srcA[2]; const u8* srcB[2];
-  #pragma unroll
-  for (int i = 0; i < 2; ++i) {
-    int ci = i * 512 + tid;
-    int r = ci >> 2;
-    int logc = (ci & 3) ^ ((r >> 1) & 3);
-    srcA[i] = A8 + (size_t)(m0 + r) * K + logc * 16;
-    srcB[i] = B8 + (size_t)(n0 + r) * K + logc * 16;
-  }
-
-  v4f acc[8][4];
-  #pragma unroll
-  for (int i = 0; i < 8; ++i)
-    #pragma unroll
-    for (int j = 0; j < 4; ++j) acc[i][j] = (v4f){0.f, 0.f, 0.f, 0.f};
-
-  const int csw = (lc >> 1) & 3;
-  int aoff[8], boff[4];
-  #pragma unroll
-  for (int mi = 0; mi < 8; ++mi) aoff[mi] = (wm * 128 + mi * 16 + lc) * 64 + ((lq ^ csw) << 4);
-  #pragma unroll
-  for (int ni = 0; ni < 4; ++ni) boff[ni] = (wn * 64 + ni * 16 + lc) * 64 + ((lq ^ csw) << 4);
-
-  auto stageA = [&](int t, int i) {
-    gload16(&lds8[(t & 1) * 32768 + i * 8192 + wid * 1024], srcA[i] + t * 64);
-  };
-  auto stageB = [&](int t, int i) {
-    gload16(&lds8[(t & 1) * 32768 + 16384 + i * 8192 + wid * 1024], srcB[i] + t * 64);
-  };
-
-  stageA(0, 0); stageA(0, 1); stageB(0, 0); stageB(0, 1);
-  stageA(1, 0); stageA(1, 1); stageB(1, 0); stageB(1, 1);
-  asm volatile("s_waitcnt vmcnt(4)" ::: "memory");
-  __builtin_amdgcn_s_barrier();
-
-  union Frag { v4i v; long long ll[2]; };
-  const int NT = K >> 6;
-  for (int t = 0; t < NT; ++t) {
-    const u8* Ab = &lds8[(t & 1) * 32768];
-    const u8* Bb = Ab + 16384;
-    Frag fa[8], fb[4];
-
-    #pragma unroll
-    for (int ni = 0; ni < 4; ++ni) fb[ni].v = *(const v4i*)(Bb + boff[ni]);
-    #pragma unroll
-    for (int mi = 0; mi < 4; ++mi) fa[mi].v = *(const v4i*)(Ab + aoff[mi]);
-    asm volatile("s_waitcnt lgkmcnt(0)" ::: "memory");
-    __builtin_amdgcn_sched_barrier(0);
-    __builtin_amdgcn_s_setprio(1);
-    #pragma unroll
-    for (int mi = 0; mi < 4; ++mi)
-      #pragma unroll
-      for (int ni = 0; ni < 4; ++ni)
-        acc[mi][ni] = __builtin_amdgcn_mfma_f32_16x16x32_fp8_fp8(fa[mi].ll[0], fb[ni].ll[0], acc[mi][ni], 0, 0, 0);
-    __builtin_amdgcn_s_setprio(0);
-    __builtin_amdgcn_s_barrier();
-
-    #pragma unroll
-    for (int mi = 0; mi < 4; ++mi) fa[mi + 4].v = *(const v4i*)(Ab + aoff[mi + 4]);
-    if (t + 2 < NT) stageB(t + 2, 0);
-    asm volatile("s_waitcnt lgkmcnt(0)" ::: "memory");
-    __builtin_amdgcn_sched_barrier(0);
-    __builtin_amdgcn_s_setprio(1);
-    #pragma unroll
-    for (int mi = 0; mi < 4; ++mi)
-      #pragma unroll
-      for (int ni = 0; ni < 4; ++ni)
-        acc[mi + 4][ni] = __builtin_amdgcn_mfma_f32_16x16x32_fp8_fp8(fa[mi + 4].ll[0], fb[ni].ll[0], acc[mi + 4][ni], 0, 0, 0);
-    __builtin_amdgcn_s_setprio(0);
-    __builtin_amdgcn_s_barrier();
-
-    if (t + 2 < NT) { stageB(t + 2, 1); stageA(t + 2, 0); }
-    __builtin_amdgcn_s_setprio(1);
-    #pragma unroll
-    for (int mi = 0; mi < 4; ++mi)
-      #pragma unroll
-      for (int ni = 0; ni < 4; ++ni)
-        acc[mi][ni] = __builtin_amdgcn_mfma_f32_16x16x32_fp8_fp8(fa[mi].ll[1], fb[ni].ll[1], acc[mi][ni], 0, 0, 0);
-    __builtin_amdgcn_s_setprio(0);
-    __builtin_amdgcn_s_barrier();
-
-    if (t + 2 < NT) stageA(t + 2, 1);
-    __builtin_amdgcn_s_setprio(1);
-    #pragma unroll
-    for (int mi = 0; mi < 4; ++mi)
-      #pragma unroll
-      for (int ni = 0; ni < 4; ++ni)
-        acc[mi + 4][ni] = __builtin_amdgcn_mfma_f32_16x16x32_fp8_fp8(fa[mi + 4].ll[1], fb[ni].ll[1], acc[mi + 4][ni], 0, 0, 0);
-    __builtin_amdgcn_s_setprio(0);
-    if (t + 2 < NT) { asm volatile("s_waitcnt vmcnt(4)" ::: "memory"); }
-    else            { asm volatile("s_waitcnt vmcnt(0)" ::: "memory"); }
-    __builtin_amdgcn_s_barrier();
-  }
-  asm volatile("s_waitcnt vmcnt(0)" ::: "memory");
-
-  #pragma unroll
-  for (int mi = 0; mi < 8; ++mi)
-    #pragma unroll
-    for (int ni = 0; ni < 4; ++ni)
-      acc[mi][ni] *= 0.015625f;
-
-  if constexpr (EPI == EPI_GLU) {
-    #pragma unroll
-    for (int mi = 0; mi < 8; ++mi)
-      #pragma unroll
-      for (int np = 0; np < 2; ++np)
-        #pragma unroll
-        for (int r = 0; r < 4; ++r) {
-          int grow = m0 + wm * 128 + mi * 16 + lq * 4 + r;
-          int gcol = (n0 >> 1) + wn * 32 + np * 16 + lc;
-          float g = acc[mi][2 * np][r];
-          float u = acc[mi][2 * np + 1][r];
-          Cbf[(size_t)grow * ldc + gcol] = f2bf(u * g / (1.0f + __expf(-g)));
+          C8[perm8((size_t)grow * ldc + gcol)] = f2fp8(u * g / (1.0f + __expf(-g)));
         }
     return;
   } else {
@@ -587,28 +426,27 @@
   }
 }
 
-template <int ASRC, int EPI>
-__launch_bounds__(256, 2)
-__global__ void k_gemm4(const u16* __restrict__ Abf, const u16* __restrict__ Bbf,
+template <int EPI>
+__launch_bounds__(256, 4)
+__global__ void k_gemm9(const u8* __restrict__ A8, const u8* __restrict__ B8,
                         u16* __restrict__ Cbf, float* __restrict__ Cf32,
-                        const int* __restrict__ keepArr, RmsSrc rs, int K, int ldb, int ldc) {
-  __shared__ __align__(16) u16 lds[2][16384];
+                        const int* __restrict__ keepArr, RmsSrc rs,
+                        int K, int ldb, int ldc) {
+  __shared__ __align__(16) u8 lds8[32768];
   const int tid = threadIdx.x;
   const int lane = tid & 63, wid = tid >> 6;
   const int wm = wid >> 1, wn = wid & 1;
   const int lc = lane & 15, lq = lane >> 4;
   const int m0 = blockIdx.x * 128, n0 = blockIdx.y * 128;
 
-  const u16* srcA[4]; const u16* srcB[4];
-  #pragma unroll
-  for (int i = 0; i < 4; ++i) {
-    int s = i * 256 + tid;
-    int row = s >> 3;
-    int c3 = (s & 7) ^ (row & 7);
-    int ar = m0 + row;
-    if constexpr (ASRC == ASRC_AOMAP) ar = (ar >> 4) * 17 + 1 + (ar & 15);
-    srcA[i] = Abf + (size_t)ar * K + c3 * 8;
-    srcB[i] = Bbf + (size_t)(n0 + row) * ldb + c3 * 8;
+  const u8* srcA[2]; const u8* srcB[2];
+  #pragma unroll
+  for (int i = 0; i < 2; ++i) {
+    int ci = i * 256 + tid;
+    int r = ci >> 2;
+    int logc = (ci & 3) ^ ((r >> 1) & 3);
+    srcA[i] = A8 + (size_t)(m0 + r) * K + logc * 16;
+    srcB[i] = B8 + (size_t)(n0 + r) * ldb + logc * 16;
   }
 
   v4f acc[4][4];
@@ -617,49 +455,46 @@
     #pragma unroll
     for (int j = 0; j < 4; ++j) acc[i][j] = (v4f){0.f, 0.f, 0.f, 0.f};
 
-  const int sw = lc & 7;
-  const int aoff0 = (((wm * 64 + lc) * 8 + 0 + lq) ^ sw) * 8;
-  const int aoff1 = (((wm * 64 + lc) * 8 + 4 + lq) ^ sw) * 8;
-  const int boff0 = (((wn * 64 + lc) * 8 + 0 + lq) ^ sw) * 8;
-  const int boff1 = (((wn * 64 + lc) * 8 + 4 + lq) ^ sw) * 8;
-
-  auto stageTo = [&](int b) {
-    u16* dA = &lds[b][0] + wid * 512;
-    u16* dB = &lds[b][8192] + wid * 512;
-    #pragma unroll
-    for (int i = 0; i < 4; ++i) { gload16(dA + i * 2048, srcA[i]); srcA[i] += 64; }
-    #pragma unroll
-    for (int i = 0; i < 4; ++i) { gload16(dB + i * 2048, srcB[i]); srcB[i] += 64; }
+  const int csw = (lc >> 1) & 3;
+  int aoff[4], boff[4];
+  #pragma unroll
+  for (int mi = 0; mi < 4; ++mi) aoff[mi] = (wm * 64 + mi * 16 + lc) * 64 + ((lq ^ csw) << 4);
+  #pragma unroll
+  for (int ni = 0; ni < 4; ++ni) boff[ni] = (wn * 64 + ni * 16 + lc) * 64 + ((lq ^ csw) << 4);
+
+  auto stageTo = [&](int b, int t) {
+    #pragma unroll
+    for (int i = 0; i < 2; ++i) {
+      gload16(&lds8[b * 16384 + i * 4096 + wid * 1024], srcA[i] + t * 64);
+      gload16(&lds8[b * 16384 + 8192 + i * 4096 + wid * 1024], srcB[i] + t * 64);
+    }
   };
 
-  stageTo(0);
+  stageTo(0, 0);
+  union Frag { v4i v; long long ll[2]; };
   const int NT = K >> 6;
   for (int t = 0; t < NT; ++t) {
     const int cur = t & 1;
     if (t + 1 < NT) {
-      stageTo(cur ^ 1);
-      asm volatile("s_waitcnt vmcnt(8)" ::: "memory");
+      stageTo(cur ^ 1, t + 1);
+      asm volatile("s_waitcnt vmcnt(4)" ::: "memory");
     } else {
       asm volatile("s_waitcnt vmcnt(0)" ::: "memory");
     }
     __builtin_amdgcn_s_barrier();
-    const u16* Ab = &lds[cur][0];
-    const u16* Bb = &lds[cur][8192];
-    v8s a0[4], a1[4], b0[4], b1[4];
-    #pragma unroll
-    for (int mi = 0; mi < 4; ++mi) a0[mi] = *(const v8s*)(Ab + aoff0 + mi * 1024);
-    #pragma unroll
-    for (int ni = 0; ni < 4; ++ni) b0[ni] = *(const v8s*)(Bb + boff0 + ni * 1024);
-    #pragma unroll
-    for (int mi = 0; mi < 4; ++mi) a1[mi] = *(const v8s*)(Ab + aoff1 + mi * 1024);
-    #pragma unroll
-    for (int ni = 0; ni < 4; ++ni) b1[ni] = *(const v8s*)(Bb + boff1 + ni * 1024);
+    const u8* Ab = &lds8[cur * 16384];
+    const u8* Bb = Ab + 8192;
+    Frag fa[4], fb[4];
+    #pragma unroll
+    for (int mi = 0; mi < 4; ++mi) fa[mi].v = *(const v4i*)(Ab + aoff[mi]);
+    #pragma unroll
+    for (int ni = 0; ni < 4; ++ni) fb[ni].v = *(const v4i*)(Bb + boff[ni]);
     __builtin_amdgcn_s_setprio(1);
     #pragma unroll
     for (int mi = 0; mi < 4; ++mi)
       #pragma unroll
       for (int ni = 0; ni < 4; ++ni)
-        acc[mi][ni] = __builtin_amdgcn_mfma_f32_16x16x32_bf16(a0[mi], b0[ni], acc[mi][ni], 0, 0, 0);
+        acc[mi][ni] = __builtin_amdgcn_mfma_f32_16x16x32_fp8_fp8(fa[mi].ll[0], fb[ni].ll[0], acc[mi][ni], 0, 0, 0);
     __builtin_amdgcn_s_setprio(0);
     asm volatile("s_waitcnt lgkmcnt(0)" ::: "memory");
     __builtin_amdgcn_sched_barrier(0);
@@ -669,7 +504,7 @@
     for (int mi = 0; mi < 4; ++mi)
       #pragma unroll
       for (int ni = 0; ni < 4; ++ni)
-        acc[mi][ni] = __builtin_amdgcn_mfma_f32_16x16x32_bf16(a1[mi], b1[ni], acc[mi][ni], 0, 0, 0);
+        acc[mi][ni] = __builtin_amdgcn_mfma_f32_16x16x32_fp8_fp8(fa[mi].ll[1], fb[ni].ll[1], acc[mi][ni], 0, 0, 0);
     __builtin_amdgcn_s_setprio(0);
   }
 
@@ -682,7 +517,7 @@
         int grow = m0 + wm * 64 + mi * 16 + lq * 4 + r;
         int gcol = n0 + wn * 64 + ni * 16 + lc;
         size_t idx = (size_t)grow * ldc + gcol;
-        float vv = acc[mi][ni][r];
+        float vv = acc[mi][ni][r] * 0.015625f;
         if constexpr (EPI == EPI_BF16) {
           Cbf[idx] = f2bf(vv);
         } else if constexpr (EPI == EPI_OEMB) {
@@ -866,7 +701,7 @@
 }
 
 __global__ void k_attn(u16* __restrict__ qb, const u16* __restrict__ kb,
-                       const u16* __restrict__ vb) {
+                       const u16* __restrict__ vb, u8* __restrict__ ao8) {
   int blk = blockIdx.x;
   int h = blk % cH, bn = blk / cH;
   __shared__ float qs[16][128], ks[17][128], vs[17][128], ps[16][18];
@@ -901,7 +736,8 @@
     int qi = e >> 7, d = e & 127;
     float s = 0.f;
     for (int kk = 0; kk < 17; ++kk) s += ps[qi][kk] * vs[kk][d];
-    qb[((size_t)(bn * 17 + 1 + qi)) * cD + h * cHD + d] = f2bf(s);
+    if (ao8) ao8[perm8((size_t)(bn * 16 + qi) * cD + h * cHD + d)] = f2fp8(s);
+    else     qb[((size_t)(bn * 17 + 1 + qi)) * cD + h * cHD + d] = f2bf(s);
   }
 }
 
@@ -1054,67 +890,67 @@
   k_select <<<dim3(cB * 16), 256, 0, stream>>>(lmask, rv, self);
   k_anchors<<<dim3(cB),      256, 0, stream>>>(lmask, self, ids, anchors, keepA, ftok, cpos);
 
-  const size_t szKV   = szQ;
-  const size_t szCbuf = (size_t)MTOK * 4096 * 2;
   size_t kvb_off  = a1off;
-  size_t a1f_off  = (kvb_off + szKV + 255) & ~(size_t)255;
-  size_t a1f_sz   = 2 * szQ > (szX + szCbuf) ? 2 * szQ : (szX + szCbuf);
+  size_t a1f_off  = (kvb_off + szQ + 255) & ~(size_t)255;
+  size_t a1f_sz   = 2 * szQ > (szX + (size_t)MTOK * 4096 * 2) ? 2 * szQ
+                                                             : (szX + (size_t)MTOK * 4096 * 2);
   size_t wreg_off = (a1f_off + a1f_sz + 255) & ~(size_t)255;
   size_t wreg_sz  = (size_t)cV * cD * 2;
   size_t need_fast = wreg_off + wreg_sz;
 
   if (need_fast <= ws_size) {
-    u16*   kvb   = (u16*)(wsb + kvb_off);
+    u8*    kv8   = (u8*)(wsb + kvb_off);
     u16*   kb    = (u16*)(wsb + a1f_off);
     u16*   vb    = (u16*)(wsb + a1f_off + szQ);
     float* xb    = (float*)(wsb + a1f_off);
-    u16*   cbuf  = (u16*)(wsb + a1f_off + szX);
+    u8*    ao8   = (u8*)(wsb + a1f_off + 2 * szQ);
+    u8*    cbuf8 = (u8*)(wsb + a1f_off + 2 * szQ + (size_t)MTOK * cD);
     v4f*   parts = (v4f*)(wsb + a1f_off);
     u8*    h8    = (u8*)(wsb + a1f_off + (size_t)16 * 1024 * 1024);
     u16*   hb    = qb;
     u16*   houtb = qb;
     u16*   wT    = (u16*)(wsb + wreg_off);
     const size_t szDD = (size_t)cD * cD;
-    u16* wqT = wT;            u16* wkT = wT + szDD;
-    u16* wvT = wT + 2 * szDD; u16* woT = wT + 3 * szDD;
+    u8* wq8 = (u8*)wT;        u8* wk8 = wq8 + szDD;
+    u8* wv8 = wq8 + 2 * szDD; u8* wo8 = wq8 + 3 * szDD;
     const size_t szDF = (size_t)cD * cDFF;
-    u8*  wgu8 = (u8*)wT;
-    u16* wdT  = wT + 2 * szDF;
-    u8*  h8m  = (u8*)(wT + 3 * szDF);
-    u8*  wlm8 = (u8*)wT;
-
-    k_build2<<<dim3(MKV), 256, 0, stream>>>(hs, emb, nattn, nchs, ftok, cpos, kvb);
-
-    k_tconv<<<dim3(32, 32), 256, 0, stream>>>(wq, wqT, cD, cD);
-    k_tconv<<<dim3(32, 32), 256, 0, stream>>>(wk, wkT, cD, cD);
-    k_tconv<<<dim3(32, 32), 256, 0, stream>>>(wv, wvT, cD, cD);
-    k_tconv<<<dim3(32, 32), 256, 0, stream>>>(wo, woT, cD, cD);
-
-    k_gemm4<ASRC_BF16, EPI_BF16><<<dim3(MKV / 128, cD / 128), 256, 0, stream>>>(
-        kvb, wqT, qb, nullptr, nullptr, rs, cD, cD, cD);
-    k_gemm4<ASRC_BF16, EPI_BF16><<<dim3(MKV / 128, cD / 128), 256, 0, stream>>>(
-        kvb, wkT, kb, nullptr, nullptr, rs, cD, cD, cD);
-    k_gemm4<ASRC_BF16, EPI_BF16><<<dim3(MKV / 128, cD / 128), 256, 0, stream>>>(
-        kvb, wvT, vb, nullptr, nullptr, rs, cD, cD, cD);
+    u8* wgu8 = (u8*)wT;
+    u8* wd8  = (u8*)wT + 2 * szDF;
+    u8* h8m  = (u8*)wT + 3 * szDF;
+    u8* wlm8 = (u8*)wT;
+
+    k_build2<<<dim3(MKV), 256, 0, stream>>>(hs, emb, nattn, nchs, ftok, cpos, kv8);
+
+    k_tconv8<<<dim3(32, 32), 256, 0, stream>>>(wq, wq8, cD, cD, -1, 64.0f);
+    k_tconv8<<<dim3(32, 32), 256, 0, stream>>>(wk, wk8, cD, cD, -1, 64.0f);
+    k_tconv8<<<dim3(32, 32), 256, 0, stream>>>(wv, wv8, cD, cD, -1, 64.0f);
+    k_tconv8<<<dim3(32, 32), 256, 0, stream>>>(wo, wo8, cD, cD, -1, 64.0f);
+
+    k_gemm9<EPI_BF16><<<dim3(MKV / 128, cD / 128), 256, 0, stream>>>(
+        kv8, wq8, qb, nullptr, nullptr, rs, cD, cD, cD);
+    k_gemm9<EPI_BF16><<<dim3(MKV / 128, cD / 128), 256, 0, stream>>>(
+        kv8, wk8, kb, nullptr, nullptr, rs, cD, cD, cD);
+    k_gemm9<EPI_BF16><<<dim3(MKV / 128, cD / 128), 256, 0, stream>>>(
+        kv8, wv8, vb, nullptr, nullptr, rs, cD, cD, cD);
 
     k_rope<<<dim3(2 * MKV), 256, 0, stream>>>(qb, kb, anchors, cpos);
-    k_attn<<<dim3(cB * cNA * cH), 64, 0, stream>>>(qb, kb, vb);
-
-    k_gemm4<ASRC_AOMAP, EPI_OEMB><<<dim3(MTOK / 128, cD / 128), 256, 0, stream>>>(
-        qb, woT, nullptr, xb, keepA, rs, cD, cD, cD);
+    k_attn<<<dim3(cB * cNA * cH), 64, 0, stream>>>(qb, kb, vb, ao8);
+
+    k_gemm9<EPI_OEMB><<<dim3(MTOK / 128, cD / 128), 256, 0, stream>>>(
+        ao8, wo8, nullptr, xb, keepA, rs, cD, cD, cD);
 
     k_rms<<<dim3(MTOK), 256, 0, stream>>>(xb, nmlp, hb);
     k_cvt8<<<dim3(1024), 256, 0, stream>>>(hb, h8m, (long)MTOK * cD);
 
     k_tconv8<<<dim3(128, 32), 256, 0, stream>>>(wg, wgu8, cD, cDFF, 0, 64.0f);
     k_tconv8<<<dim3(128, 32), 256, 0, stream>>>(wu, wgu8, cD, cDFF, 16, 64.0f);
-    k_tconv <<<dim3(32, 128), 256, 0, stream>>>(wd, wdT, cDFF, cD);
+    k_tconv8<<<dim3(32, 128), 256, 0, stream>>>(wd, wd8, cDFF, cD, -1, 64.0f);
 
     for (int cb = 0; cb < cDFF; cb += 4096) {
       k_gemm8<EPI_GLU><<<dim3(MTOK / 256, 32), 512, 0, stream>>>(
-          h8m, wgu8 + (size_t)cb * 2 * cD, cbuf, nullptr, cD, 4096, 0);
-      k_gemm4<ASRC_BF16, EPI_DOWNACC><<<dim3(MTOK / 128, cD / 128), 256, 0, stream>>>(
-          cbuf, wdT + cb, nullptr, xb, nullptr, rs, 4096, cDFF, cD);
+          h8m, wgu8 + (size_t)cb * 2 * cD, cbuf8, nullptr, cD, 4096, 0);
+      k_gemm9<EPI_DOWNACC><<<dim3(MTOK / 128, cD / 128), 256, 0, stream>>>(
+          cbuf8, wd8 + cb, nullptr, xb, nullptr, rs, 4096, cDFF, cD);
     }
 
     k_rms<<<dim3(MTOK), 256, 0, stream>>>(xb, nout, houtb);
@@ -1163,7 +999,7 @@
       nullptr, wv, vb, nullptr, nullptr, nullptr, nullptr, rs, cD, cD, cD);
 
   k_rope<<<dim3(2 * MKV), 256, 0, stream>>>(qb, kb, anchors, cpos);
-  k_attn<<<dim3(cB * cNA * cH), 64, 0, stream>>>(qb, kb, vb);
+  k_attn<<<dim3(cB * cNA * cH), 64, 0, stream>>>(qb, kb, vb, nullptr);
 
   k_gemm<ASRC_AOMAP, 0, EPI_OEMB><<<dim3(MTOK / 128, cD / 128), 256, 0, stream>>>(
       qb, wo, nullptr, xb, nullptr, keepA, nullptr, rs, cD, cD, cD);
```
